# Kernel tuning notes

Measured on AMD Instinct MI355X. Metric: run time of the kernel, lower is better.

## Reference

```python
import jax, jax.numpy as jnp
import numpy as np

B, N, C, H = 8, 1024, 768, 12
HD = C // H
SCALE = HD ** -0.5
LAMBD = 4.0
N_ITERS = 5


def setup_inputs() -> dict:
    key = jax.random.key(0)
    k1, k2, k3, k4, k5 = jax.random.split(key, 5)
    x = jax.random.normal(k1, (B, N, C), dtype=jnp.float32)
    W_qkv = jax.random.normal(k2, (C, 2 * C), dtype=jnp.float32) * (C ** -0.5)
    b_qkv = jax.random.normal(k3, (2 * C,), dtype=jnp.float32) * 0.02
    W_proj = jax.random.normal(k4, (C, C), dtype=jnp.float32) * (C ** -0.5)
    b_proj = jax.random.normal(k5, (C,), dtype=jnp.float32) * 0.02
    return {"x": x, "W_qkv": W_qkv, "b_qkv": b_qkv, "W_proj": W_proj, "b_proj": b_proj}


def _soft_threshold(s, t):
    # (s - t) where s >= t, (s + t) where s <= -t, else 0  (matches the int-mask math)
    return jnp.where(s >= t, s - t, jnp.where(s <= -t, s + t, jnp.zeros_like(s)))


def reference(x, W_qkv, b_qkv, W_proj, b_proj):
    qkv = (x @ W_qkv + b_qkv).reshape(B, N, 2, H, HD)
    qkv = jnp.transpose(qkv, (2, 0, 3, 1, 4))  # [2, B, H, N, HD]
    k, v = qkv[0], qkv[1]

    # mu: [B, H, 1, 1], scalar per (batch, head): N*C/4 / ||k||_1
    mu = (N * C / 4.0) / jnp.sum(jnp.abs(k), axis=(-1, -2), keepdims=True)
    lm = LAMBD * mu

    l = jnp.zeros((B, H, N, HD), dtype=x.dtype)
    y = jnp.zeros((B, H, N, HD), dtype=x.dtype)

    for _ in range(N_ITERS):
        s = _soft_threshold(k - l + y / mu, lm)
        k2 = k - s - y / mu
        attn = jax.nn.softmax(jnp.einsum('bhnd,bhmd->bhnm', k2, k2) * SCALE, axis=-1)
        l = jnp.einsum('bhnm,bhmd->bhnd', attn, v)
        y = y + mu * (k - l - s)

    s = _soft_threshold(k - l + y / mu, lm)
    k2 = k - s - y / mu
    attn = jax.nn.softmax(jnp.einsum('bhnd,bhmd->bhnm', k2, k2) * SCALE, axis=-1)
    out = jnp.einsum('bhnm,bhmd->bhnd', attn, v)  # [B, H, N, HD]

    out = jnp.transpose(out, (0, 2, 1, 3)).reshape(B, N, C)
    out = out @ W_proj + b_proj
    return out, attn
```

## Files before the change

kernel.cpp:

```cpp
#include <hip/hip_runtime.h>

#define B_   8
#define N_   1024
#define C_   768
#define H_   12
#define HD_  64
#define BH_  96
#define SCALE_ 0.125f
#define NIT_ 5

typedef __attribute__((ext_vector_type(8))) short bfrag;
typedef __attribute__((ext_vector_type(4))) float facc;

__device__ __forceinline__ unsigned short bfhi(float x)
{
    return (unsigned short)(__float_as_uint(x) >> 16);
}
__device__ __forceinline__ unsigned short bflo(float x)
{
    const unsigned hu = __float_as_uint(x) & 0xffff0000u;
    return (unsigned short)(__float_as_uint(x - __uint_as_float(hu)) >> 16);
}
__device__ __forceinline__ bfrag pack_hi(float4 a, float4 b)
{
    bfrag r;
    r[0] = (short)bfhi(a.x); r[1] = (short)bfhi(a.y);
    r[2] = (short)bfhi(a.z); r[3] = (short)bfhi(a.w);
    r[4] = (short)bfhi(b.x); r[5] = (short)bfhi(b.y);
    r[6] = (short)bfhi(b.z); r[7] = (short)bfhi(b.w);
    return r;
}
__device__ __forceinline__ bfrag pack_lo(float4 a, float4 b)
{
    bfrag r;
    r[0] = (short)bflo(a.x); r[1] = (short)bflo(a.y);
    r[2] = (short)bflo(a.z); r[3] = (short)bflo(a.w);
    r[4] = (short)bflo(b.x); r[5] = (short)bflo(b.y);
    r[6] = (short)bflo(b.z); r[7] = (short)bflo(b.w);
    return r;
}

__global__ __launch_bounds__(256)
void split_flat(const float* __restrict__ In,
                unsigned short* __restrict__ Oh, unsigned short* __restrict__ Ol)
{
    const size_t i = ((size_t)blockIdx.x * 256 + threadIdx.x) * 8;
    const float4 a = *(const float4*)(In + i);
    const float4 b = *(const float4*)(In + i + 4);
    *(bfrag*)(Oh + i) = pack_hi(a, b);
    *(bfrag*)(Ol + i) = pack_lo(a, b);
}

__global__ __launch_bounds__(256)
void split_wt(const float* __restrict__ W, int ncols,
              unsigned short* __restrict__ Th, unsigned short* __restrict__ Tl)
{
    __shared__ float Ts[64][68];
    const int tid = threadIdx.x;
    const int c0 = blockIdx.x * 64;
    const int k0 = blockIdx.y * 64;

    {
        int e = tid;
#pragma unroll
        for (int t = 0; t < 4; ++t, e += 256) {
            const int r = e >> 4, c4 = (e & 15) << 2;
            *(float4*)&Ts[r][c4] =
                *(const float4*)(W + (size_t)(k0 + r) * ncols + c0 + c4);
        }
    }
    __syncthreads();

#pragma unroll
    for (int t = 0; t < 2; ++t) {
        const int idx = t * 2048 + tid * 8;
        const int cr = idx >> 6, ck = idx & 63;
        bfrag h8, l8;
#pragma unroll
        for (int q = 0; q < 8; ++q) {
            const float v = Ts[ck + q][cr];
            h8[q] = (short)bfhi(v);
            l8[q] = (short)bflo(v);
        }
        const size_t go = (size_t)(c0 + cr) * 768 + k0 + ck;
        *(bfrag*)(Th + go) = h8;
        *(bfrag*)(Tl + go) = l8;
    }
}

__global__ __launch_bounds__(256)
void qkv_mfma(const unsigned short* __restrict__ Xh, const unsigned short* __restrict__ Xl,
              const unsigned short* __restrict__ Wth, const unsigned short* __restrict__ Wtl,
              const float* __restrict__ bias,
              float* __restrict__ Kb, float* __restrict__ Vb)
{
    __shared__ short Ahs[64][72];
    __shared__ short Als[64][72];
    __shared__ short Bhs[64][72];
    __shared__ short Bls[64][72];

    const int tid  = threadIdx.x;
    const int lane = tid & 63;
    const int w    = tid >> 6;
    const int g    = lane >> 4;
    const int r16  = lane & 15;
    const int m0   = blockIdx.y * 64;
    const int c0   = blockIdx.x * 64;

    facc o0 = {0.f, 0.f, 0.f, 0.f};
    facc o1 = {0.f, 0.f, 0.f, 0.f};
    facc o2 = {0.f, 0.f, 0.f, 0.f};
    facc o3 = {0.f, 0.f, 0.f, 0.f};

    const int i0 = tid * 8,        r0 = i0 >> 6, cc0 = i0 & 63;
    const int i1 = 2048 + tid * 8, r1 = i1 >> 6, cc1 = i1 & 63;

    bfrag ta0 = *(const bfrag*)(Xh + (size_t)(m0 + r0) * 768 + cc0);
    bfrag ta1 = *(const bfrag*)(Xh + (size_t)(m0 + r1) * 768 + cc1);
    bfrag tb0 = *(const bfrag*)(Xl + (size_t)(m0 + r0) * 768 + cc0);
    bfrag tb1 = *(const bfrag*)(Xl + (size_t)(m0 + r1) * 768 + cc1);
    bfrag tw0 = *(const bfrag*)(Wth + (size_t)(c0 + r0) * 768 + cc0);
    bfrag tw1 = *(const bfrag*)(Wth + (size_t)(c0 + r1) * 768 + cc1);
    bfrag tz0 = *(const bfrag*)(Wtl + (size_t)(c0 + r0) * 768 + cc0);
    bfrag tz1 = *(const bfrag*)(Wtl + (size_t)(c0 + r1) * 768 + cc1);

    for (int ks = 0; ks < 12; ++ks) {
        __syncthreads();
        *(bfrag*)&Ahs[r0][cc0] = ta0;  *(bfrag*)&Ahs[r1][cc1] = ta1;
        *(bfrag*)&Als[r0][cc0] = tb0;  *(bfrag*)&Als[r1][cc1] = tb1;
        *(bfrag*)&Bhs[r0][cc0] = tw0;  *(bfrag*)&Bhs[r1][cc1] = tw1;
        *(bfrag*)&Bls[r0][cc0] = tz0;  *(bfrag*)&Bls[r1][cc1] = tz1;
        if (ks + 1 < 12) {
            const int kn = (ks + 1) * 64;
            ta0 = *(const bfrag*)(Xh + (size_t)(m0 + r0) * 768 + kn + cc0);
            ta1 = *(const bfrag*)(Xh + (size_t)(m0 + r1) * 768 + kn + cc1);
            tb0 = *(const bfrag*)(Xl + (size_t)(m0 + r0) * 768 + kn + cc0);
            tb1 = *(const bfrag*)(Xl + (size_t)(m0 + r1) * 768 + kn + cc1);
            tw0 = *(const bfrag*)(Wth + (size_t)(c0 + r0) * 768 + kn + cc0);
            tw1 = *(const bfrag*)(Wth + (size_t)(c0 + r1) * 768 + kn + cc1);
            tz0 = *(const bfrag*)(Wtl + (size_t)(c0 + r0) * 768 + kn + cc0);
            tz1 = *(const bfrag*)(Wtl + (size_t)(c0 + r1) * 768 + kn + cc1);
        }
        __syncthreads();

        const bfrag ah0 = *(const bfrag*)&Ahs[16 * w + r16][8 * g];
        const bfrag ah1 = *(const bfrag*)&Ahs[16 * w + r16][32 + 8 * g];
        const bfrag al0 = *(const bfrag*)&Als[16 * w + r16][8 * g];
        const bfrag al1 = *(const bfrag*)&Als[16 * w + r16][32 + 8 * g];
        {
            bfrag b0 = *(const bfrag*)&Bhs[r16][8 * g];
            bfrag b1 = *(const bfrag*)&Bhs[r16][32 + 8 * g];
            bfrag c1 = *(const bfrag*)&Bls[r16][8 * g];
            bfrag c2 = *(const bfrag*)&Bls[r16][32 + 8 * g];
            o0 = __builtin_amdgcn_mfma_f32_16x16x32_bf16(ah0, b0, o0, 0, 0, 0);
            o0 = __builtin_amdgcn_mfma_f32_16x16x32_bf16(al0, b0, o0, 0, 0, 0);
            o0 = __builtin_amdgcn_mfma_f32_16x16x32_bf16(ah0, c1, o0, 0, 0, 0);
            o0 = __builtin_amdgcn_mfma_f32_16x16x32_bf16(ah1, b1, o0, 0, 0, 0);
            o0 = __builtin_amdgcn_mfma_f32_16x16x32_bf16(al1, b1, o0, 0, 0, 0);
            o0 = __builtin_amdgcn_mfma_f32_16x16x32_bf16(ah1, c2, o0, 0, 0, 0);
        }
        {
            bfrag b0 = *(const bfrag*)&Bhs[16 + r16][8 * g];
            bfrag b1 = *(const bfrag*)&Bhs[16 + r16][32 + 8 * g];
            bfrag c1 = *(const bfrag*)&Bls[16 + r16][8 * g];
            bfrag c2 = *(const bfrag*)&Bls[16 + r16][32 + 8 * g];
            o1 = __builtin_amdgcn_mfma_f32_16x16x32_bf16(ah0, b0, o1, 0, 0, 0);
            o1 = __builtin_amdgcn_mfma_f32_16x16x32_bf16(al0, b0, o1, 0, 0, 0);
            o1 = __builtin_amdgcn_mfma_f32_16x16x32_bf16(ah0, c1, o1, 0, 0, 0);
            o1 = __builtin_amdgcn_mfma_f32_16x16x32_bf16(ah1, b1, o1, 0, 0, 0);
            o1 = __builtin_amdgcn_mfma_f32_16x16x32_bf16(al1, b1, o1, 0, 0, 0);
            o1 = __builtin_amdgcn_mfma_f32_16x16x32_bf16(ah1, c2, o1, 0, 0, 0);
        }
        {
            bfrag b0 = *(const bfrag*)&Bhs[32 + r16][8 * g];
            bfrag b1 = *(const bfrag*)&Bhs[32 + r16][32 + 8 * g];
            bfrag c1 = *(const bfrag*)&Bls[32 + r16][8 * g];
            bfrag c2 = *(const bfrag*)&Bls[32 + r16][32 + 8 * g];
            o2 = __builtin_amdgcn_mfma_f32_16x16x32_bf16(ah0, b0, o2, 0, 0, 0);
            o2 = __builtin_amdgcn_mfma_f32_16x16x32_bf16(al0, b0, o2, 0, 0, 0);
            o2 = __builtin_amdgcn_mfma_f32_16x16x32_bf16(ah0, c1, o2, 0, 0, 0);
            o2 = __builtin_amdgcn_mfma_f32_16x16x32_bf16(ah1, b1, o2, 0, 0, 0);
            o2 = __builtin_amdgcn_mfma_f32_16x16x32_bf16(al1, b1, o2, 0, 0, 0);
            o2 = __builtin_amdgcn_mfma_f32_16x16x32_bf16(ah1, c2, o2, 0, 0, 0);
        }
        {
            bfrag b0 = *(const bfrag*)&Bhs[48 + r16][8 * g];
            bfrag b1 = *(const bfrag*)&Bhs[48 + r16][32 + 8 * g];
            bfrag c1 = *(const bfrag*)&Bls[48 + r16][8 * g];
            bfrag c2 = *(const bfrag*)&Bls[48 + r16][32 + 8 * g];
            o3 = __builtin_amdgcn_mfma_f32_16x16x32_bf16(ah0, b0, o3, 0, 0, 0);
            o3 = __builtin_amdgcn_mfma_f32_16x16x32_bf16(al0, b0, o3, 0, 0, 0);
            o3 = __builtin_amdgcn_mfma_f32_16x16x32_bf16(ah0, c1, o3, 0, 0, 0);
            o3 = __builtin_amdgcn_mfma_f32_16x16x32_bf16(ah1, b1, o3, 0, 0, 0);
            o3 = __builtin_amdgcn_mfma_f32_16x16x32_bf16(al1, b1, o3, 0, 0, 0);
            o3 = __builtin_amdgcn_mfma_f32_16x16x32_bf16(ah1, c2, o3, 0, 0, 0);
        }
    }

    const int h = (c0 % C_) >> 6;
    float* tgt = (c0 < C_) ? Kb : Vb;
    const float bb0 = bias[c0 + r16];
    const float bb1 = bias[c0 + 16 + r16];
    const float bb2 = bias[c0 + 32 + r16];
    const float bb3 = bias[c0 + 48 + r16];

    const int mrow = m0 + 16 * w + 4 * g;
    const int bidx = mrow >> 10;
    const int nidx = mrow & 1023;
    float* trow = tgt + ((size_t)(bidx * H_ + h) * N_ + nidx) * HD_ + r16;
    trow[0 * HD_ + 0]  = o0.x + bb0; trow[0 * HD_ + 16] = o1.x + bb1;
    trow[0 * HD_ + 32] = o2.x + bb2; trow[0 * HD_ + 48] = o3.x + bb3;
    trow[1 * HD_ + 0]  = o0.y + bb0; trow[1 * HD_ + 16] = o1.y + bb1;
    trow[1 * HD_ + 32] = o2.y + bb2; trow[1 * HD_ + 48] = o3.y + bb3;
    trow[2 * HD_ + 0]  = o0.z + bb0; trow[2 * HD_ + 16] = o1.z + bb1;
    trow[2 * HD_ + 32] = o2.z + bb2; trow[2 * HD_ + 48] = o3.z + bb3;
    trow[3 * HD_ + 0]  = o0.w + bb0; trow[3 * HD_ + 16] = o1.w + bb1;
    trow[3 * HD_ + 32] = o2.w + bb2; trow[3 * HD_ + 48] = o3.w + bb3;
}

__global__ __launch_bounds__(256)
void proj_mfma(const unsigned short* __restrict__ Lh, const unsigned short* __restrict__ Ll,
               const unsigned short* __restrict__ Wth, const unsigned short* __restrict__ Wtl,
               const float* __restrict__ bias, float* __restrict__ Out)
{
    __shared__ short Ahs[64][72];
    __shared__ short Als[64][72];
    __shared__ short Bhs[64][72];
    __shared__ short Bls[64][72];

    const int tid  = threadIdx.x;
    const int lane = tid & 63;
    const int w    = tid >> 6;
    const int g    = lane >> 4;
    const int r16  = lane & 15;
    const int m0   = blockIdx.y * 64;
    const int c0   = blockIdx.x * 64;

    facc o0 = {0.f, 0.f, 0.f, 0.f};
    facc o1 = {0.f, 0.f, 0.f, 0.f};
    facc o2 = {0.f, 0.f, 0.f, 0.f};
    facc o3 = {0.f, 0.f, 0.f, 0.f};

    const int i0 = tid * 8,        r0 = i0 >> 6, cc0 = i0 & 63;
    const int i1 = 2048 + tid * 8, r1 = i1 >> 6, cc1 = i1 & 63;
    const int t0 = m0 + r0, ab0 = t0 >> 10, an0 = t0 & 1023;
    const int t1 = m0 + r1, ab1 = t1 >> 10, an1 = t1 & 1023;

    bfrag ta0 = *(const bfrag*)(Lh + ((size_t)(ab0 * H_) * N_ + an0) * HD_ + cc0);
    bfrag ta1 = *(const bfrag*)(Lh + ((size_t)(ab1 * H_) * N_ + an1) * HD_ + cc1);
    bfrag tb0 = *(const bfrag*)(Ll + ((size_t)(ab0 * H_) * N_ + an0) * HD_ + cc0);
    bfrag tb1 = *(const bfrag*)(Ll + ((size_t)(ab1 * H_) * N_ + an1) * HD_ + cc1);
    bfrag tw0 = *(const bfrag*)(Wth + (size_t)(c0 + r0) * 768 + cc0);
    bfrag tw1 = *(const bfrag*)(Wth + (size_t)(c0 + r1) * 768 + cc1);
    bfrag tz0 = *(const bfrag*)(Wtl + (size_t)(c0 + r0) * 768 + cc0);
    bfrag tz1 = *(const bfrag*)(Wtl + (size_t)(c0 + r1) * 768 + cc1);

    for (int ks = 0; ks < 12; ++ks) {
        __syncthreads();
        *(bfrag*)&Ahs[r0][cc0] = ta0;  *(bfrag*)&Ahs[r1][cc1] = ta1;
        *(bfrag*)&Als[r0][cc0] = tb0;  *(bfrag*)&Als[r1][cc1] = tb1;
        *(bfrag*)&Bhs[r0][cc0] = tw0;  *(bfrag*)&Bhs[r1][cc1] = tw1;
        *(bfrag*)&Bls[r0][cc0] = tz0;  *(bfrag*)&Bls[r1][cc1] = tz1;
        if (ks + 1 < 12) {
            const int kn = ks + 1;
            const size_t ga0 = ((size_t)(ab0 * H_ + kn) * N_ + an0) * HD_ + cc0;
            const size_t ga1 = ((size_t)(ab1 * H_ + kn) * N_ + an1) * HD_ + cc1;
            ta0 = *(const bfrag*)(Lh + ga0);
            ta1 = *(const bfrag*)(Lh + ga1);
            tb0 = *(const bfrag*)(Ll + ga0);
            tb1 = *(const bfrag*)(Ll + ga1);
            tw0 = *(const bfrag*)(Wth + (size_t)(c0 + r0) * 768 + kn * 64 + cc0);
            tw1 = *(const bfrag*)(Wth + (size_t)(c0 + r1) * 768 + kn * 64 + cc1);
            tz0 = *(const bfrag*)(Wtl + (size_t)(c0 + r0) * 768 + kn * 64 + cc0);
            tz1 = *(const bfrag*)(Wtl + (size_t)(c0 + r1) * 768 + kn * 64 + cc1);
        }
        __syncthreads();

        const bfrag ah0 = *(const bfrag*)&Ahs[16 * w + r16][8 * g];
        const bfrag ah1 = *(const bfrag*)&Ahs[16 * w + r16][32 + 8 * g];
        const bfrag al0 = *(const bfrag*)&Als[16 * w + r16][8 * g];
        const bfrag al1 = *(const bfrag*)&Als[16 * w + r16][32 + 8 * g];
        {
            bfrag b0 = *(const bfrag*)&Bhs[r16][8 * g];
            bfrag b1 = *(const bfrag*)&Bhs[r16][32 + 8 * g];
            bfrag c1 = *(const bfrag*)&Bls[r16][8 * g];
            bfrag c2 = *(const bfrag*)&Bls[r16][32 + 8 * g];
            o0 = __builtin_amdgcn_mfma_f32_16x16x32_bf16(ah0, b0, o0, 0, 0, 0);
            o0 = __builtin_amdgcn_mfma_f32_16x16x32_bf16(al0, b0, o0, 0, 0, 0);
            o0 = __builtin_amdgcn_mfma_f32_16x16x32_bf16(ah0, c1, o0, 0, 0, 0);
            o0 = __builtin_amdgcn_mfma_f32_16x16x32_bf16(ah1, b1, o0, 0, 0, 0);
            o0 = __builtin_amdgcn_mfma_f32_16x16x32_bf16(al1, b1, o0, 0, 0, 0);
            o0 = __builtin_amdgcn_mfma_f32_16x16x32_bf16(ah1, c2, o0, 0, 0, 0);
        }
        {
            bfrag b0 = *(const bfrag*)&Bhs[16 + r16][8 * g];
            bfrag b1 = *(const bfrag*)&Bhs[16 + r16][32 + 8 * g];
            bfrag c1 = *(const bfrag*)&Bls[16 + r16][8 * g];
            bfrag c2 = *(const bfrag*)&Bls[16 + r16][32 + 8 * g];
            o1 = __builtin_amdgcn_mfma_f32_16x16x32_bf16(ah0, b0, o1, 0, 0, 0);
            o1 = __builtin_amdgcn_mfma_f32_16x16x32_bf16(al0, b0, o1, 0, 0, 0);
            o1 = __builtin_amdgcn_mfma_f32_16x16x32_bf16(ah0, c1, o1, 0, 0, 0);
            o1 = __builtin_amdgcn_mfma_f32_16x16x32_bf16(ah1, b1, o1, 0, 0, 0);
            o1 = __builtin_amdgcn_mfma_f32_16x16x32_bf16(al1, b1, o1, 0, 0, 0);
            o1 = __builtin_amdgcn_mfma_f32_16x16x32_bf16(ah1, c2, o1, 0, 0, 0);
        }
        {
            bfrag b0 = *(const bfrag*)&Bhs[32 + r16][8 * g];
            bfrag b1 = *(const bfrag*)&Bhs[32 + r16][32 + 8 * g];
            bfrag c1 = *(const bfrag*)&Bls[32 + r16][8 * g];
            bfrag c2 = *(const bfrag*)&Bls[32 + r16][32 + 8 * g];
            o2 = __builtin_amdgcn_mfma_f32_16x16x32_bf16(ah0, b0, o2, 0, 0, 0);
            o2 = __builtin_amdgcn_mfma_f32_16x16x32_bf16(al0, b0, o2, 0, 0, 0);
            o2 = __builtin_amdgcn_mfma_f32_16x16x32_bf16(ah0, c1, o2, 0, 0, 0);
            o2 = __builtin_amdgcn_mfma_f32_16x16x32_bf16(ah1, b1, o2, 0, 0, 0);
            o2 = __builtin_amdgcn_mfma_f32_16x16x32_bf16(al1, b1, o2, 0, 0, 0);
            o2 = __builtin_amdgcn_mfma_f32_16x16x32_bf16(ah1, c2, o2, 0, 0, 0);
        }
        {
            bfrag b0 = *(const bfrag*)&Bhs[48 + r16][8 * g];
            bfrag b1 = *(const bfrag*)&Bhs[48 + r16][32 + 8 * g];
            bfrag c1 = *(const bfrag*)&Bls[48 + r16][8 * g];
            bfrag c2 = *(const bfrag*)&Bls[48 + r16][32 + 8 * g];
            o3 = __builtin_amdgcn_mfma_f32_16x16x32_bf16(ah0, b0, o3, 0, 0, 0);
            o3 = __builtin_amdgcn_mfma_f32_16x16x32_bf16(al0, b0, o3, 0, 0, 0);
            o3 = __builtin_amdgcn_mfma_f32_16x16x32_bf16(ah0, c1, o3, 0, 0, 0);
            o3 = __builtin_amdgcn_mfma_f32_16x16x32_bf16(ah1, b1, o3, 0, 0, 0);
            o3 = __builtin_amdgcn_mfma_f32_16x16x32_bf16(al1, b1, o3, 0, 0, 0);
            o3 = __builtin_amdgcn_mfma_f32_16x16x32_bf16(ah1, c2, o3, 0, 0, 0);
        }
    }

    const float bb0 = bias[c0 + r16];
    const float bb1 = bias[c0 + 16 + r16];
    const float bb2 = bias[c0 + 32 + r16];
    const float bb3 = bias[c0 + 48 + r16];
    float* orow = Out + (size_t)(m0 + 16 * w + 4 * g) * C_ + c0 + r16;
    orow[0 * C_ + 0]  = o0.x + bb0; orow[0 * C_ + 16] = o1.x + bb1;
    orow[0 * C_ + 32] = o2.x + bb2; orow[0 * C_ + 48] = o3.x + bb3;
    orow[1 * C_ + 0]  = o0.y + bb0; orow[1 * C_ + 16] = o1.y + bb1;
    orow[1 * C_ + 32] = o2.y + bb2; orow[1 * C_ + 48] = o3.y + bb3;
    orow[2 * C_ + 0]  = o0.z + bb0; orow[2 * C_ + 16] = o1.z + bb1;
    orow[2 * C_ + 32] = o2.z + bb2; orow[2 * C_ + 48] = o3.z + bb3;
    orow[3 * C_ + 0]  = o0.w + bb0; orow[3 * C_ + 16] = o1.w + bb1;
    orow[3 * C_ + 32] = o2.w + bb2; orow[3 * C_ + 48] = o3.w + bb3;
}

__global__ __launch_bounds__(256)
void musum(const float* __restrict__ Kb, float* __restrict__ mu)
{
    const int bh = blockIdx.x;
    const int tid = threadIdx.x;
    const float* p = Kb + (size_t)bh * (N_ * HD_);
    float s = 0.0f;
    for (int i = tid; i < N_ * HD_; i += 256) s += fabsf(p[i]);
    for (int off = 32; off; off >>= 1) s += __shfl_down(s, off, 64);
    __shared__ float red[4];
    if ((tid & 63) == 0) red[tid >> 6] = s;
    __syncthreads();
    if (tid == 0)
        mu[bh] = (float)(N_ * C_ / 4.0) / (red[0] + red[1] + red[2] + red[3]);
}

__global__ __launch_bounds__(256)
void ew_fused(const float* __restrict__ Kb, const float* __restrict__ Lb,
              float* __restrict__ Yb, const float* __restrict__ mu,
              float* __restrict__ K2b,
              unsigned short* __restrict__ K2h, unsigned short* __restrict__ K2l,
              int upd)
{
    const int i = blockIdx.x * 256 + threadIdx.x;
    const int bh = i >> 16;
    const float m = mu[bh];
    const float lm = 4.0f * m;
    const float lv = Lb[i];
    float y = Yb[i];
    if (upd) {
        y = 2.0f * y + m * (K2b[i] - lv);
        Yb[i] = y;
    }
    const float yom = y / m;
    const float kv = Kb[i];
    const float t = kv - lv + yom;
    const float s = (t >= lm) ? (t - lm) : ((t <= -lm) ? (t + lm) : 0.0f);
    const float k2 = kv - s - yom;
    K2b[i] = k2;
    K2h[i] = bfhi(k2);
    K2l[i] = bflo(k2);
}

__global__ __launch_bounds__(256)
void vt_split(const float* __restrict__ Vb,
              unsigned short* __restrict__ Vth, unsigned short* __restrict__ Vtl)
{
    __shared__ float Ts[64][68];
    const int tid = threadIdx.x;
    const int bh = blockIdx.y;
    const int n0 = blockIdx.x * 64;
    const float* vb = Vb + ((size_t)bh * N_ + n0) * HD_;

    {
        int e = tid;
#pragma unroll
        for (int t = 0; t < 4; ++t, e += 256) {
            const int r = e >> 4, c4 = (e & 15) << 2;
            *(float4*)&Ts[r][c4] = *(const float4*)(vb + r * HD_ + c4);
        }
    }
    __syncthreads();

#pragma unroll
    for (int t = 0; t < 2; ++t) {
        const int idx = t * 2048 + tid * 8;
        const int d = idx >> 6, c = idx & 63;
        bfrag h8, l8;
#pragma unroll
        for (int q = 0; q < 8; ++q) {
            const float v = Ts[c + q][d];
            h8[q] = (short)bfhi(v);
            l8[q] = (short)bflo(v);
        }
        const size_t go = ((size_t)bh * HD_ + d) * N_ + n0 + c;
        *(bfrag*)(Vth + go) = h8;
        *(bfrag*)(Vtl + go) = l8;
    }
}

__global__ __launch_bounds__(256)
void flash(const unsigned short* __restrict__ K2h, const unsigned short* __restrict__ K2l,
           const unsigned short* __restrict__ Vth, const unsigned short* __restrict__ Vtl,
           float* __restrict__ Lout, float* __restrict__ Mrow, float* __restrict__ Zrow)
{
    __shared__ short Kh[64][72];
    __shared__ short Kl[64][72];
    __shared__ short Vh[64][72];
    __shared__ short Vl[64][72];
    short (&Ph)[64][72] = Kh;
    short (&Pl)[64][72] = Kl;

    const int tid  = threadIdx.x;
    const int lane = tid & 63;
    const int w    = tid >> 6;
    const int g    = lane >> 4;
    const int r16  = lane & 15;
    const int bh   = blockIdx.y;
    const int q0   = blockIdx.x * 64;

    const unsigned short* kh = K2h + (size_t)bh * (N_ * HD_);
    const unsigned short* kl = K2l + (size_t)bh * (N_ * HD_);
    const unsigned short* vh = Vth + (size_t)bh * (N_ * HD_);
    const unsigned short* vl = Vtl + (size_t)bh * (N_ * HD_);

    const size_t qoff = (size_t)(q0 + 16 * w + r16) * HD_ + 8 * g;
    const bfrag qh0 = *(const bfrag*)(kh + qoff);
    const bfrag qh1 = *(const bfrag*)(kh + qoff + 32);
    const bfrag ql0 = *(const bfrag*)(kl + qoff);
    const bfrag ql1 = *(const bfrag*)(kl + qoff + 32);

    const int i0 = tid * 8,        r0 = i0 >> 6, cc0 = i0 & 63;
    const int i1 = 2048 + tid * 8, r1 = i1 >> 6, cc1 = i1 & 63;

    bfrag pk0 = *(const bfrag*)(kh + i0);
    bfrag pk1 = *(const bfrag*)(kh + i1);
    bfrag pm0 = *(const bfrag*)(kl + i0);
    bfrag pm1 = *(const bfrag*)(kl + i1);

    float mr0 = -1e30f, mr1 = -1e30f, mr2 = -1e30f, mr3 = -1e30f;
    float zr0 = 0.0f,  zr1 = 0.0f,  zr2 = 0.0f,  zr3 = 0.0f;
    facc o0 = {0.f, 0.f, 0.f, 0.f};
    facc o1 = {0.f, 0.f, 0.f, 0.f};
    facc o2 = {0.f, 0.f, 0.f, 0.f};
    facc o3 = {0.f, 0.f, 0.f, 0.f};

    for (int kt = 0; kt < 16; ++kt) {
        __syncthreads();
        *(bfrag*)&Kh[r0][cc0] = pk0;  *(bfrag*)&Kh[r1][cc1] = pk1;
        *(bfrag*)&Kl[r0][cc0] = pm0;  *(bfrag*)&Kl[r1][cc1] = pm1;
        const bfrag tv0 = *(const bfrag*)(vh + (size_t)r0 * N_ + kt * 64 + cc0);
        const bfrag tv1 = *(const bfrag*)(vh + (size_t)r1 * N_ + kt * 64 + cc1);
        const bfrag tw0 = *(const bfrag*)(vl + (size_t)r0 * N_ + kt * 64 + cc0);
        const bfrag tw1 = *(const bfrag*)(vl + (size_t)r1 * N_ + kt * 64 + cc1);
        if (kt + 1 < 16) {
            const size_t gn = (size_t)(kt + 1) * 4096;
            pk0 = *(const bfrag*)(kh + gn + i0);
            pk1 = *(const bfrag*)(kh + gn + i1);
            pm0 = *(const bfrag*)(kl + gn + i0);
            pm1 = *(const bfrag*)(kl + gn + i1);
        }
        __syncthreads();

        facc s0 = {0.f, 0.f, 0.f, 0.f};
        facc s1 = {0.f, 0.f, 0.f, 0.f};
        facc s2 = {0.f, 0.f, 0.f, 0.f};
        facc s3 = {0.f, 0.f, 0.f, 0.f};
        {
            bfrag b0 = *(const bfrag*)&Kh[r16][8 * g];
            bfrag b1 = *(const bfrag*)&Kh[r16][32 + 8 * g];
            bfrag c0 = *(const bfrag*)&Kl[r16][8 * g];
            bfrag c1 = *(const bfrag*)&Kl[r16][32 + 8 * g];
            s0 = __builtin_amdgcn_mfma_f32_16x16x32_bf16(qh0, b0, s0, 0, 0, 0);
            s0 = __builtin_amdgcn_mfma_f32_16x16x32_bf16(ql0, b0, s0, 0, 0, 0);
            s0 = __builtin_amdgcn_mfma_f32_16x16x32_bf16(qh0, c0, s0, 0, 0, 0);
            s0 = __builtin_amdgcn_mfma_f32_16x16x32_bf16(qh1, b1, s0, 0, 0, 0);
            s0 = __builtin_amdgcn_mfma_f32_16x16x32_bf16(ql1, b1, s0, 0, 0, 0);
            s0 = __builtin_amdgcn_mfma_f32_16x16x32_bf16(qh1, c1, s0, 0, 0, 0);
        }
        {
            bfrag b0 = *(const bfrag*)&Kh[16 + r16][8 * g];
            bfrag b1 = *(const bfrag*)&Kh[16 + r16][32 + 8 * g];
            bfrag c0 = *(const bfrag*)&Kl[16 + r16][8 * g];
            bfrag c1 = *(const bfrag*)&Kl[16 + r16][32 + 8 * g];
            s1 = __builtin_amdgcn_mfma_f32_16x16x32_bf16(qh0, b0, s1, 0, 0, 0);
            s1 = __builtin_amdgcn_mfma_f32_16x16x32_bf16(ql0, b0, s1, 0, 0, 0);
            s1 = __builtin_amdgcn_mfma_f32_16x16x32_bf16(qh0, c0, s1, 0, 0, 0);
            s1 = __builtin_amdgcn_mfma_f32_16x16x32_bf16(qh1, b1, s1, 0, 0, 0);
            s1 = __builtin_amdgcn_mfma_f32_16x16x32_bf16(ql1, b1, s1, 0, 0, 0);
            s1 = __builtin_amdgcn_mfma_f32_16x16x32_bf16(qh1, c1, s1, 0, 0, 0);
        }
        {
            bfrag b0 = *(const bfrag*)&Kh[32 + r16][8 * g];
            bfrag b1 = *(const bfrag*)&Kh[32 + r16][32 + 8 * g];
            bfrag c0 = *(const bfrag*)&Kl[32 + r16][8 * g];
            bfrag c1 = *(const bfrag*)&Kl[32 + r16][32 + 8 * g];
            s2 = __builtin_amdgcn_mfma_f32_16x16x32_bf16(qh0, b0, s2, 0, 0, 0);
            s2 = __builtin_amdgcn_mfma_f32_16x16x32_bf16(ql0, b0, s2, 0, 0, 0);
            s2 = __builtin_amdgcn_mfma_f32_16x16x32_bf16(qh0, c0, s2, 0, 0, 0);
            s2 = __builtin_amdgcn_mfma_f32_16x16x32_bf16(qh1, b1, s2, 0, 0, 0);
            s2 = __builtin_amdgcn_mfma_f32_16x16x32_bf16(ql1, b1, s2, 0, 0, 0);
            s2 = __builtin_amdgcn_mfma_f32_16x16x32_bf16(qh1, c1, s2, 0, 0, 0);
        }
        {
            bfrag b0 = *(const bfrag*)&Kh[48 + r16][8 * g];
            bfrag b1 = *(const bfrag*)&Kh[48 + r16][32 + 8 * g];
            bfrag c0 = *(const bfrag*)&Kl[48 + r16][8 * g];
            bfrag c1 = *(const bfrag*)&Kl[48 + r16][32 + 8 * g];
            s3 = __builtin_amdgcn_mfma_f32_16x16x32_bf16(qh0, b0, s3, 0, 0, 0);
            s3 = __builtin_amdgcn_mfma_f32_16x16x32_bf16(ql0, b0, s3, 0, 0, 0);
            s3 = __builtin_amdgcn_mfma_f32_16x16x32_bf16(qh0, c0, s3, 0, 0, 0);
            s3 = __builtin_amdgcn_mfma_f32_16x16x32_bf16(qh1, b1, s3, 0, 0, 0);
            s3 = __builtin_amdgcn_mfma_f32_16x16x32_bf16(ql1, b1, s3, 0, 0, 0);
            s3 = __builtin_amdgcn_mfma_f32_16x16x32_bf16(qh1, c1, s3, 0, 0, 0);
        }

        s0 = s0 * SCALE_;  s1 = s1 * SCALE_;  s2 = s2 * SCALE_;  s3 = s3 * SCALE_;

        float mt0 = fmaxf(fmaxf(s0.x, s1.x), fmaxf(s2.x, s3.x));
        float mt1 = fmaxf(fmaxf(s0.y, s1.y), fmaxf(s2.y, s3.y));
        float mt2 = fmaxf(fmaxf(s0.z, s1.z), fmaxf(s2.z, s3.z));
        float mt3 = fmaxf(fmaxf(s0.w, s1.w), fmaxf(s2.w, s3.w));
        for (int off = 8; off; off >>= 1) {
            mt0 = fmaxf(mt0, __shfl_xor(mt0, off, 16));
            mt1 = fmaxf(mt1, __shfl_xor(mt1, off, 16));
            mt2 = fmaxf(mt2, __shfl_xor(mt2, off, 16));
            mt3 = fmaxf(mt3, __shfl_xor(mt3, off, 16));
        }
        const float mn0 = fmaxf(mr0, mt0), mn1 = fmaxf(mr1, mt1);
        const float mn2 = fmaxf(mr2, mt2), mn3 = fmaxf(mr3, mt3);
        const float a0 = __expf(mr0 - mn0), a1 = __expf(mr1 - mn1);
        const float a2 = __expf(mr2 - mn2), a3 = __expf(mr3 - mn3);
        mr0 = mn0; mr1 = mn1; mr2 = mn2; mr3 = mn3;

        const float pa0 = __expf(s0.x - mn0), pa1 = __expf(s0.y - mn1);
        const float pa2 = __expf(s0.z - mn2), pa3 = __expf(s0.w - mn3);
        const float pb0 = __expf(s1.x - mn0), pb1 = __expf(s1.y - mn1);
        const float pb2 = __expf(s1.z - mn2), pb3 = __expf(s1.w - mn3);
        const float pc0 = __expf(s2.x - mn0), pc1 = __expf(s2.y - mn1);
        const float pc2 = __expf(s2.z - mn2), pc3 = __expf(s2.w - mn3);
        const float pd0 = __expf(s3.x - mn0), pd1 = __expf(s3.y - mn1);
        const float pd2 = __expf(s3.z - mn2), pd3 = __expf(s3.w - mn3);

        float zs0 = pa0 + pb0 + pc0 + pd0;
        float zs1 = pa1 + pb1 + pc1 + pd1;
        float zs2 = pa2 + pb2 + pc2 + pd2;
        float zs3 = pa3 + pb3 + pc3 + pd3;
        for (int off = 8; off; off >>= 1) {
            zs0 += __shfl_xor(zs0, off, 16);
            zs1 += __shfl_xor(zs1, off, 16);
            zs2 += __shfl_xor(zs2, off, 16);
            zs3 += __shfl_xor(zs3, off, 16);
        }
        zr0 = zr0 * a0 + zs0;  zr1 = zr1 * a1 + zs1;
        zr2 = zr2 * a2 + zs2;  zr3 = zr3 * a3 + zs3;

        o0.x *= a0; o0.y *= a1; o0.z *= a2; o0.w *= a3;
        o1.x *= a0; o1.y *= a1; o1.z *= a2; o1.w *= a3;
        o2.x *= a0; o2.y *= a1; o2.z *= a2; o2.w *= a3;
        o3.x *= a0; o3.y *= a1; o3.z *= a2; o3.w *= a3;

        *(bfrag*)&Vh[r0][cc0] = tv0;  *(bfrag*)&Vh[r1][cc1] = tv1;
        *(bfrag*)&Vl[r0][cc0] = tw0;  *(bfrag*)&Vl[r1][cc1] = tw1;

        __syncthreads();

        {
            const int pr = 16 * w + 4 * g;
            Ph[pr + 0][r16]      = (short)bfhi(pa0); Pl[pr + 0][r16]      = (short)bflo(pa0);
            Ph[pr + 1][r16]      = (short)bfhi(pa1); Pl[pr + 1][r16]      = (short)bflo(pa1);
            Ph[pr + 2][r16]      = (short)bfhi(pa2); Pl[pr + 2][r16]      = (short)bflo(pa2);
            Ph[pr + 3][r16]      = (short)bfhi(pa3); Pl[pr + 3][r16]      = (short)bflo(pa3);
            Ph[pr + 0][16 + r16] = (short)bfhi(pb0); Pl[pr + 0][16 + r16] = (short)bflo(pb0);
            Ph[pr + 1][16 + r16] = (short)bfhi(pb1); Pl[pr + 1][16 + r16] = (short)bflo(pb1);
            Ph[pr + 2][16 + r16] = (short)bfhi(pb2); Pl[pr + 2][16 + r16] = (short)bflo(pb2);
            Ph[pr + 3][16 + r16] = (short)bfhi(pb3); Pl[pr + 3][16 + r16] = (short)bflo(pb3);
            Ph[pr + 0][32 + r16] = (short)bfhi(pc0); Pl[pr + 0][32 + r16] = (short)bflo(pc0);
            Ph[pr + 1][32 + r16] = (short)bfhi(pc1); Pl[pr + 1][32 + r16] = (short)bflo(pc1);
            Ph[pr + 2][32 + r16] = (short)bfhi(pc2); Pl[pr + 2][32 + r16] = (short)bflo(pc2);
            Ph[pr + 3][32 + r16] = (short)bfhi(pc3); Pl[pr + 3][32 + r16] = (short)bflo(pc3);
            Ph[pr + 0][48 + r16] = (short)bfhi(pd0); Pl[pr + 0][48 + r16] = (short)bflo(pd0);
            Ph[pr + 1][48 + r16] = (short)bfhi(pd1); Pl[pr + 1][48 + r16] = (short)bflo(pd1);
            Ph[pr + 2][48 + r16] = (short)bfhi(pd2); Pl[pr + 2][48 + r16] = (short)bflo(pd2);
            Ph[pr + 3][48 + r16] = (short)bfhi(pd3); Pl[pr + 3][48 + r16] = (short)bflo(pd3);
        }
        __builtin_amdgcn_wave_barrier();

        {
            const bfrag ph0 = *(const bfrag*)&Ph[16 * w + r16][8 * g];
            const bfrag ph1 = *(const bfrag*)&Ph[16 * w + r16][32 + 8 * g];
            const bfrag pl0 = *(const bfrag*)&Pl[16 * w + r16][8 * g];
            const bfrag pl1 = *(const bfrag*)&Pl[16 * w + r16][32 + 8 * g];
            {
                bfrag b0 = *(const bfrag*)&Vh[r16][8 * g];
                bfrag b1 = *(const bfrag*)&Vh[r16][32 + 8 * g];
                bfrag c0 = *(const bfrag*)&Vl[r16][8 * g];
                bfrag c1 = *(const bfrag*)&Vl[r16][32 + 8 * g];
                o0 = __builtin_amdgcn_mfma_f32_16x16x32_bf16(ph0, b0, o0, 0, 0, 0);
                o0 = __builtin_amdgcn_mfma_f32_16x16x32_bf16(pl0, b0, o0, 0, 0, 0);
                o0 = __builtin_amdgcn_mfma_f32_16x16x32_bf16(ph0, c0, o0, 0, 0, 0);
                o0 = __builtin_amdgcn_mfma_f32_16x16x32_bf16(ph1, b1, o0, 0, 0, 0);
                o0 = __builtin_amdgcn_mfma_f32_16x16x32_bf16(pl1, b1, o0, 0, 0, 0);
                o0 = __builtin_amdgcn_mfma_f32_16x16x32_bf16(ph1, c1, o0, 0, 0, 0);
            }
            {
                bfrag b0 = *(const bfrag*)&Vh[16 + r16][8 * g];
                bfrag b1 = *(const bfrag*)&Vh[16 + r16][32 + 8 * g];
                bfrag c0 = *(const bfrag*)&Vl[16 + r16][8 * g];
                bfrag c1 = *(const bfrag*)&Vl[16 + r16][32 + 8 * g];
                o1 = __builtin_amdgcn_mfma_f32_16x16x32_bf16(ph0, b0, o1, 0, 0, 0);
                o1 = __builtin_amdgcn_mfma_f32_16x16x32_bf16(pl0, b0, o1, 0, 0, 0);
                o1 = __builtin_amdgcn_mfma_f32_16x16x32_bf16(ph0, c0, o1, 0, 0, 0);
                o1 = __builtin_amdgcn_mfma_f32_16x16x32_bf16(ph1, b1, o1, 0, 0, 0);
                o1 = __builtin_amdgcn_mfma_f32_16x16x32_bf16(pl1, b1, o1, 0, 0, 0);
                o1 = __builtin_amdgcn_mfma_f32_16x16x32_bf16(ph1, c1, o1, 0, 0, 0);
            }
            {
                bfrag b0 = *(const bfrag*)&Vh[32 + r16][8 * g];
                bfrag b1 = *(const bfrag*)&Vh[32 + r16][32 + 8 * g];
                bfrag c0 = *(const bfrag*)&Vl[32 + r16][8 * g];
                bfrag c1 = *(const bfrag*)&Vl[32 + r16][32 + 8 * g];
                o2 = __builtin_amdgcn_mfma_f32_16x16x32_bf16(ph0, b0, o2, 0, 0, 0);
                o2 = __builtin_amdgcn_mfma_f32_16x16x32_bf16(pl0, b0, o2, 0, 0, 0);
                o2 = __builtin_amdgcn_mfma_f32_16x16x32_bf16(ph0, c0, o2, 0, 0, 0);
                o2 = __builtin_amdgcn_mfma_f32_16x16x32_bf16(ph1, b1, o2, 0, 0, 0);
                o2 = __builtin_amdgcn_mfma_f32_16x16x32_bf16(pl1, b1, o2, 0, 0, 0);
                o2 = __builtin_amdgcn_mfma_f32_16x16x32_bf16(ph1, c1, o2, 0, 0, 0);
            }
            {
                bfrag b0 = *(const bfrag*)&Vh[48 + r16][8 * g];
                bfrag b1 = *(const bfrag*)&Vh[48 + r16][32 + 8 * g];
                bfrag c0 = *(const bfrag*)&Vl[48 + r16][8 * g];
                bfrag c1 = *(const bfrag*)&Vl[48 + r16][32 + 8 * g];
                o3 = __builtin_amdgcn_mfma_f32_16x16x32_bf16(ph0, b0, o3, 0, 0, 0);
                o3 = __builtin_amdgcn_mfma_f32_16x16x32_bf16(pl0, b0, o3, 0, 0, 0);
                o3 = __builtin_amdgcn_mfma_f32_16x16x32_bf16(ph0, c0, o3, 0, 0, 0);
                o3 = __builtin_amdgcn_mfma_f32_16x16x32_bf16(ph1, b1, o3, 0, 0, 0);
                o3 = __builtin_amdgcn_mfma_f32_16x16x32_bf16(pl1, b1, o3, 0, 0, 0);
                o3 = __builtin_amdgcn_mfma_f32_16x16x32_bf16(ph1, c1, o3, 0, 0, 0);
            }
        }
    }

    const float zi0 = 1.0f / zr0, zi1 = 1.0f / zr1;
    const float zi2 = 1.0f / zr2, zi3 = 1.0f / zr3;
    float* lrow = Lout + ((size_t)bh * N_ + q0 + 16 * w + 4 * g) * HD_ + r16;
    lrow[0 * HD_ + 0]  = o0.x * zi0; lrow[0 * HD_ + 16] = o1.x * zi0;
    lrow[0 * HD_ + 32] = o2.x * zi0; lrow[0 * HD_ + 48] = o3.x * zi0;
    lrow[1 * HD_ + 0]  = o0.y * zi1; lrow[1 * HD_ + 16] = o1.y * zi1;
    lrow[1 * HD_ + 32] = o2.y * zi1; lrow[1 * HD_ + 48] = o3.y * zi1;
    lrow[2 * HD_ + 0]  = o0.z * zi2; lrow[2 * HD_ + 16] = o1.z * zi2;
    lrow[2 * HD_ + 32] = o2.z * zi2; lrow[2 * HD_ + 48] = o3.z * zi2;
    lrow[3 * HD_ + 0]  = o0.w * zi3; lrow[3 * HD_ + 16] = o1.w * zi3;
    lrow[3 * HD_ + 32] = o2.w * zi3; lrow[3 * HD_ + 48] = o3.w * zi3;

    if (r16 == 0) {
        const size_t rb = (size_t)bh * N_ + q0 + 16 * w + 4 * g;
        Mrow[rb + 0] = mr0; Mrow[rb + 1] = mr1;
        Mrow[rb + 2] = mr2; Mrow[rb + 3] = mr3;
        Zrow[rb + 0] = zr0; Zrow[rb + 1] = zr1;
        Zrow[rb + 2] = zr2; Zrow[rb + 3] = zr3;
    }
}

__global__ __launch_bounds__(256)
void attn_out_mfma(const float* __restrict__ K2v, const float* __restrict__ Mrow,
                   const float* __restrict__ Zrow, float* __restrict__ A)
{
    __shared__ short Kh[64][72];
    __shared__ short Kl[64][72];

    const int tid  = threadIdx.x;
    const int lane = tid & 63;
    const int w    = tid >> 6;
    const int g    = lane >> 4;
    const int r16  = lane & 15;
    const int bh   = blockIdx.y;
    const int q0   = blockIdx.x * 64;
    const float* k2b = K2v + (size_t)bh * N_ * HD_;

    const int qrow = q0 + 16 * w + r16;
    const float4 f0 = *(const float4*)(k2b + (size_t)qrow * HD_ + 8 * g);
    const float4 f1 = *(const float4*)(k2b + (size_t)qrow * HD_ + 8 * g + 4);
    const float4 f2 = *(const float4*)(k2b + (size_t)qrow * HD_ + 32 + 8 * g);
    const float4 f3 = *(const float4*)(k2b + (size_t)qrow * HD_ + 32 + 8 * g + 4);
    const bfrag qh0 = pack_hi(f0, f1), ql0 = pack_lo(f0, f1);
    const bfrag qh1 = pack_hi(f2, f3), ql1 = pack_lo(f2, f3);

    const size_t mb = (size_t)bh * N_ + q0 + 16 * w + 4 * g;
    const float mi0 = Mrow[mb + 0], mi1 = Mrow[mb + 1];
    const float mi2 = Mrow[mb + 2], mi3 = Mrow[mb + 3];
    const float zi0 = 1.0f / Zrow[mb + 0], zi1 = 1.0f / Zrow[mb + 1];
    const float zi2 = 1.0f / Zrow[mb + 2], zi3 = 1.0f / Zrow[mb + 3];

    const int i0 = tid * 8,        r0 = i0 >> 6, cc0 = i0 & 63;
    const int i1 = 2048 + tid * 8, r1 = i1 >> 6, cc1 = i1 & 63;

    float4 a0 = *(const float4*)(k2b + (size_t)r0 * HD_ + cc0);
    float4 a1 = *(const float4*)(k2b + (size_t)r0 * HD_ + cc0 + 4);
    float4 b0v = *(const float4*)(k2b + (size_t)r1 * HD_ + cc1);
    float4 b1v = *(const float4*)(k2b + (size_t)r1 * HD_ + cc1 + 4);

    for (int kt = 0; kt < 16; ++kt) {
        __syncthreads();
        *(bfrag*)&Kh[r0][cc0] = pack_hi(a0, a1);
        *(bfrag*)&Kl[r0][cc0] = pack_lo(a0, a1);
        *(bfrag*)&Kh[r1][cc1] = pack_hi(b0v, b1v);
        *(bfrag*)&Kl[r1][cc1] = pack_lo(b0v, b1v);
        if (kt + 1 < 16) {
            const size_t gn = (size_t)(kt + 1) * 64;
            a0  = *(const float4*)(k2b + (gn + r0) * HD_ + cc0);
            a1  = *(const float4*)(k2b + (gn + r0) * HD_ + cc0 + 4);
            b0v = *(const float4*)(k2b + (gn + r1) * HD_ + cc1);
            b1v = *(const float4*)(k2b + (gn + r1) * HD_ + cc1 + 4);
        }
        __syncthreads();

        facc s0 = {0.f, 0.f, 0.f, 0.f};
        facc s1 = {0.f, 0.f, 0.f, 0.f};
        facc s2 = {0.f, 0.f, 0.f, 0.f};
        facc s3 = {0.f, 0.f, 0.f, 0.f};
        {
            bfrag b0 = *(const bfrag*)&Kh[r16][8 * g];
            bfrag b1 = *(const bfrag*)&Kh[r16][32 + 8 * g];
            bfrag c0 = *(const bfrag*)&Kl[r16][8 * g];
            bfrag c1 = *(const bfrag*)&Kl[r16][32 + 8 * g];
            s0 = __builtin_amdgcn_mfma_f32_16x16x32_bf16(qh0, b0, s0, 0, 0, 0);
            s0 = __builtin_amdgcn_mfma_f32_16x16x32_bf16(ql0, b0, s0, 0, 0, 0);
            s0 = __builtin_amdgcn_mfma_f32_16x16x32_bf16(qh0, c0, s0, 0, 0, 0);
            s0 = __builtin_amdgcn_mfma_f32_16x16x32_bf16(qh1, b1, s0, 0, 0, 0);
            s0 = __builtin_amdgcn_mfma_f32_16x16x32_bf16(ql1, b1, s0, 0, 0, 0);
            s0 = __builtin_amdgcn_mfma_f32_16x16x32_bf16(qh1, c1, s0, 0, 0, 0);
        }
        {
            bfrag b0 = *(const bfrag*)&Kh[16 + r16][8 * g];
            bfrag b1 = *(const bfrag*)&Kh[16 + r16][32 + 8 * g];
            bfrag c0 = *(const bfrag*)&Kl[16 + r16][8 * g];
            bfrag c1 = *(const bfrag*)&Kl[16 + r16][32 + 8 * g];
            s1 = __builtin_amdgcn_mfma_f32_16x16x32_bf16(qh0, b0, s1, 0, 0, 0);
            s1 = __builtin_amdgcn_mfma_f32_16x16x32_bf16(ql0, b0, s1, 0, 0, 0);
            s1 = __builtin_amdgcn_mfma_f32_16x16x32_bf16(qh0, c0, s1, 0, 0, 0);
            s1 = __builtin_amdgcn_mfma_f32_16x16x32_bf16(qh1, b1, s1, 0, 0, 0);
            s1 = __builtin_amdgcn_mfma_f32_16x16x32_bf16(ql1, b1, s1, 0, 0, 0);
            s1 = __builtin_amdgcn_mfma_f32_16x16x32_bf16(qh1, c1, s1, 0, 0, 0);
        }
        {
            bfrag b0 = *(const bfrag*)&Kh[32 + r16][8 * g];
            bfrag b1 = *(const bfrag*)&Kh[32 + r16][32 + 8 * g];
            bfrag c0 = *(const bfrag*)&Kl[32 + r16][8 * g];
            bfrag c1 = *(const bfrag*)&Kl[32 + r16][32 + 8 * g];
            s2 = __builtin_amdgcn_mfma_f32_16x16x32_bf16(qh0, b0, s2, 0, 0, 0);
            s2 = __builtin_amdgcn_mfma_f32_16x16x32_bf16(ql0, b0, s2, 0, 0, 0);
            s2 = __builtin_amdgcn_mfma_f32_16x16x32_bf16(qh0, c0, s2, 0, 0, 0);
            s2 = __builtin_amdgcn_mfma_f32_16x16x32_bf16(qh1, b1, s2, 0, 0, 0);
            s2 = __builtin_amdgcn_mfma_f32_16x16x32_bf16(ql1, b1, s2, 0, 0, 0);
            s2 = __builtin_amdgcn_mfma_f32_16x16x32_bf16(qh1, c1, s2, 0, 0, 0);
        }
        {
            bfrag b0 = *(const bfrag*)&Kh[48 + r16][8 * g];
            bfrag b1 = *(const bfrag*)&Kh[48 + r16][32 + 8 * g];
            bfrag c0 = *(const bfrag*)&Kl[48 + r16][8 * g];
            bfrag c1 = *(const bfrag*)&Kl[48 + r16][32 + 8 * g];
            s3 = __builtin_amdgcn_mfma_f32_16x16x32_bf16(qh0, b0, s3, 0, 0, 0);
            s3 = __builtin_amdgcn_mfma_f32_16x16x32_bf16(ql0, b0, s3, 0, 0, 0);
            s3 = __builtin_amdgcn_mfma_f32_16x16x32_bf16(qh0, c0, s3, 0, 0, 0);
            s3 = __builtin_amdgcn_mfma_f32_16x16x32_bf16(qh1, b1, s3, 0, 0, 0);
            s3 = __builtin_amdgcn_mfma_f32_16x16x32_bf16(ql1, b1, s3, 0, 0, 0);
            s3 = __builtin_amdgcn_mfma_f32_16x16x32_bf16(qh1, c1, s3, 0, 0, 0);
        }

        s0 = s0 * SCALE_;  s1 = s1 * SCALE_;  s2 = s2 * SCALE_;  s3 = s3 * SCALE_;

        float* ar0 = A + (mb + 0) * N_ + kt * 64;
        float* ar1 = A + (mb + 1) * N_ + kt * 64;
        float* ar2 = A + (mb + 2) * N_ + kt * 64;
        float* ar3 = A + (mb + 3) * N_ + kt * 64;
        ar0[r16]      = __expf(s0.x - mi0) * zi0;
        ar0[16 + r16] = __expf(s1.x - mi0) * zi0;
        ar0[32 + r16] = __expf(s2.x - mi0) * zi0;
        ar0[48 + r16] = __expf(s3.x - mi0) * zi0;
        ar1[r16]      = __expf(s0.y - mi1) * zi1;
        ar1[16 + r16] = __expf(s1.y - mi1) * zi1;
        ar1[32 + r16] = __expf(s2.y - mi1) * zi1;
        ar1[48 + r16] = __expf(s3.y - mi1) * zi1;
        ar2[r16]      = __expf(s0.z - mi2) * zi2;
        ar2[16 + r16] = __expf(s1.z - mi2) * zi2;
        ar2[32 + r16] = __expf(s2.z - mi2) * zi2;
        ar2[48 + r16] = __expf(s3.z - mi2) * zi2;
        ar3[r16]      = __expf(s0.w - mi3) * zi3;
        ar3[16 + r16] = __expf(s1.w - mi3) * zi3;
        ar3[32 + r16] = __expf(s2.w - mi3) * zi3;
        ar3[48 + r16] = __expf(s3.w - mi3) * zi3;
    }
}

extern "C" void kernel_launch(void* const* d_in, const int* in_sizes, int n_in,
                              void* d_out, int out_size, void* d_ws, size_t ws_size,
                              hipStream_t stream)
{
    (void)in_sizes; (void)n_in; (void)out_size; (void)ws_size;

    const float* x  = (const float*)d_in[0];
    const float* Wq = (const float*)d_in[1];
    const float* bq = (const float*)d_in[2];
    const float* Wp = (const float*)d_in[3];
    const float* bp = (const float*)d_in[4];

    float* out_f  = (float*)d_out;
    float* attn_f = out_f + (size_t)B_ * N_ * C_;

    const size_t SZ = (size_t)BH_ * N_ * HD_;
    float* ws   = (float*)d_ws;
    float* kb   = ws;
    float* vb   = ws + SZ;
    float* lb   = ws + 2 * SZ;
    float* yb   = ws + 3 * SZ;
    float* k2b  = ws + 4 * SZ;
    float* mu   = ws + 5 * SZ;
    float* rowm = mu + 128;
    float* rowz = rowm + (size_t)BH_ * N_;

    unsigned short* k2h  = (unsigned short*)attn_f;
    unsigned short* k2l  = k2h + SZ;
    unsigned short* vth  = k2h + 2 * SZ;
    unsigned short* vtl  = k2h + 3 * SZ;
    unsigned short* xh   = k2h + 4 * SZ;
    unsigned short* xl   = k2h + 5 * SZ;
    unsigned short* wqth = k2h + 6 * SZ;
    unsigned short* wqtl = k2h + 7 * SZ;
    unsigned short* wpth = k2h + 8 * SZ;
    unsigned short* wptl = k2h + 9 * SZ;
    unsigned short* lbh  = k2h + 10 * SZ;
    unsigned short* lbl  = k2h + 11 * SZ;

    hipMemsetAsync(lb, 0, SZ * sizeof(float), stream);
    hipMemsetAsync(yb, 0, SZ * sizeof(float), stream);

    split_flat<<<3072, 256, 0, stream>>>(x, xh, xl);
    split_wt<<<dim3(24, 12), 256, 0, stream>>>(Wq, 2 * C_, wqth, wqtl);
    split_wt<<<dim3(12, 12), 256, 0, stream>>>(Wp, C_, wpth, wptl);

    qkv_mfma<<<dim3(24, 128), 256, 0, stream>>>(xh, xl, wqth, wqtl, bq, kb, vb);
    vt_split<<<dim3(16, 96), 256, 0, stream>>>(vb, vth, vtl);
    musum<<<96, 256, 0, stream>>>(kb, mu);

    for (int it = 0; it <= NIT_; ++it) {
        ew_fused<<<24576, 256, 0, stream>>>(kb, lb, yb, mu, k2b, k2h, k2l,
                                            it > 0 ? 1 : 0);
        flash<<<dim3(16, 96), 256, 0, stream>>>(k2h, k2l, vth, vtl, lb, rowm, rowz);
    }

    split_flat<<<3072, 256, 0, stream>>>(lb, lbh, lbl);
    proj_mfma<<<dim3(12, 128), 256, 0, stream>>>(lbh, lbl, wpth, wptl, bp, out_f);
    attn_out_mfma<<<dim3(16, 96), 256, 0, stream>>>(k2b, rowm, rowz, attn_f);
}
```

Before: 1.645 ms.

## Process 128 query rows per flash block and fuse final L split into flash

The flash kernel now computes two 64-row query tiles per workgroup, so each staged K/V tile in shared memory is reused twice and global K/V traffic is halved. The grid shrinks to 8x96 blocks, which raises register pressure and lowers the number of resident blocks. The last iteration writes the bf16 hi/lo split of L directly, removing the separate split_flat launch. The first ew_fused pass zeroes Y and skips reading L and Y, replacing the two memsets.

```diff
diff --git a/kernel.cpp b/kernel.cpp
--- a/kernel.cpp
+++ b/kernel.cpp
@@ -372,17 +372,22 @@
     const int bh = i >> 16;
     const float m = mu[bh];
     const float lm = 4.0f * m;
-    const float lv = Lb[i];
-    float y = Yb[i];
+    const float kv = Kb[i];
+    float k2;
     if (upd) {
-        y = 2.0f * y + m * (K2b[i] - lv);
+        const float lv = Lb[i];
+        const float y = 2.0f * Yb[i] + m * (K2b[i] - lv);
         Yb[i] = y;
-    }
-    const float yom = y / m;
-    const float kv = Kb[i];
-    const float t = kv - lv + yom;
-    const float s = (t >= lm) ? (t - lm) : ((t <= -lm) ? (t + lm) : 0.0f);
-    const float k2 = kv - s - yom;
+        const float yom = y / m;
+        const float t = kv - lv + yom;
+        const float s = (t >= lm) ? (t - lm) : ((t <= -lm) ? (t + lm) : 0.0f);
+        k2 = kv - s - yom;
+    } else {
+        Yb[i] = 0.0f;
+        const float t = kv;
+        const float s = (t >= lm) ? (t - lm) : ((t <= -lm) ? (t + lm) : 0.0f);
+        k2 = kv - s;
+    }
     K2b[i] = k2;
     K2h[i] = bfhi(k2);
     K2l[i] = bflo(k2);
@@ -428,7 +433,8 @@
 __global__ __launch_bounds__(256)
 void flash(const unsigned short* __restrict__ K2h, const unsigned short* __restrict__ K2l,
            const unsigned short* __restrict__ Vth, const unsigned short* __restrict__ Vtl,
-           float* __restrict__ Lout, float* __restrict__ Mrow, float* __restrict__ Zrow)
+           float* __restrict__ Lout, float* __restrict__ Mrow, float* __restrict__ Zrow,
+           unsigned short* __restrict__ Lbh, unsigned short* __restrict__ Lbl, int wsplit)
 {
     __shared__ short Kh[64][72];
     __shared__ short Kl[64][72];
@@ -443,18 +449,23 @@
     const int g    = lane >> 4;
     const int r16  = lane & 15;
     const int bh   = blockIdx.y;
-    const int q0   = blockIdx.x * 64;
+    const int q0   = blockIdx.x * 128;
 
     const unsigned short* kh = K2h + (size_t)bh * (N_ * HD_);
     const unsigned short* kl = K2l + (size_t)bh * (N_ * HD_);
     const unsigned short* vh = Vth + (size_t)bh * (N_ * HD_);
     const unsigned short* vl = Vtl + (size_t)bh * (N_ * HD_);
 
-    const size_t qoff = (size_t)(q0 + 16 * w + r16) * HD_ + 8 * g;
-    const bfrag qh0 = *(const bfrag*)(kh + qoff);
-    const bfrag qh1 = *(const bfrag*)(kh + qoff + 32);
-    const bfrag ql0 = *(const bfrag*)(kl + qoff);
-    const bfrag ql1 = *(const bfrag*)(kl + qoff + 32);
+    const size_t qoffA = (size_t)(q0 + 16 * w + r16) * HD_ + 8 * g;
+    const size_t qoffB = (size_t)(q0 + 64 + 16 * w + r16) * HD_ + 8 * g;
+    const bfrag qhA0 = *(const bfrag*)(kh + qoffA);
+    const bfrag qhA1 = *(const bfrag*)(kh + qoffA + 32);
+    const bfrag qlA0 = *(const bfrag*)(kl + qoffA);
+    const bfrag qlA1 = *(const bfrag*)(kl + qoffA + 32);
+    const bfrag qhB0 = *(const bfrag*)(kh + qoffB);
+    const bfrag qhB1 = *(const bfrag*)(kh + qoffB + 32);
+    const bfrag qlB0 = *(const bfrag*)(kl + qoffB);
+    const bfrag qlB1 = *(const bfrag*)(kl + qoffB + 32);
 
     const int i0 = tid * 8,        r0 = i0 >> 6, cc0 = i0 & 63;
     const int i1 = 2048 + tid * 8, r1 = i1 >> 6, cc1 = i1 & 63;
@@ -464,12 +475,18 @@
     bfrag pm0 = *(const bfrag*)(kl + i0);
     bfrag pm1 = *(const bfrag*)(kl + i1);
 
-    float mr0 = -1e30f, mr1 = -1e30f, mr2 = -1e30f, mr3 = -1e30f;
-    float zr0 = 0.0f,  zr1 = 0.0f,  zr2 = 0.0f,  zr3 = 0.0f;
-    facc o0 = {0.f, 0.f, 0.f, 0.f};
-    facc o1 = {0.f, 0.f, 0.f, 0.f};
-    facc o2 = {0.f, 0.f, 0.f, 0.f};
-    facc o3 = {0.f, 0.f, 0.f, 0.f};
+    float mrA0 = -1e30f, mrA1 = -1e30f, mrA2 = -1e30f, mrA3 = -1e30f;
+    float zrA0 = 0.0f,  zrA1 = 0.0f,  zrA2 = 0.0f,  zrA3 = 0.0f;
+    float mrB0 = -1e30f, mrB1 = -1e30f, mrB2 = -1e30f, mrB3 = -1e30f;
+    float zrB0 = 0.0f,  zrB1 = 0.0f,  zrB2 = 0.0f,  zrB3 = 0.0f;
+    facc oA0 = {0.f, 0.f, 0.f, 0.f};
+    facc oA1 = {0.f, 0.f, 0.f, 0.f};
+    facc oA2 = {0.f, 0.f, 0.f, 0.f};
+    facc oA3 = {0.f, 0.f, 0.f, 0.f};
+    facc oB0 = {0.f, 0.f, 0.f, 0.f};
+    facc oB1 = {0.f, 0.f, 0.f, 0.f};
+    facc oB2 = {0.f, 0.f, 0.f, 0.f};
+    facc oB3 = {0.f, 0.f, 0.f, 0.f};
 
     for (int kt = 0; kt < 16; ++kt) {
         __syncthreads();
@@ -488,130 +505,197 @@
         }
         __syncthreads();
 
-        facc s0 = {0.f, 0.f, 0.f, 0.f};
-        facc s1 = {0.f, 0.f, 0.f, 0.f};
-        facc s2 = {0.f, 0.f, 0.f, 0.f};
-        facc s3 = {0.f, 0.f, 0.f, 0.f};
+        facc sA0 = {0.f, 0.f, 0.f, 0.f};
+        facc sA1 = {0.f, 0.f, 0.f, 0.f};
+        facc sA2 = {0.f, 0.f, 0.f, 0.f};
+        facc sA3 = {0.f, 0.f, 0.f, 0.f};
+        facc sB0 = {0.f, 0.f, 0.f, 0.f};
+        facc sB1 = {0.f, 0.f, 0.f, 0.f};
+        facc sB2 = {0.f, 0.f, 0.f, 0.f};
+        facc sB3 = {0.f, 0.f, 0.f, 0.f};
         {
             bfrag b0 = *(const bfrag*)&Kh[r16][8 * g];
             bfrag b1 = *(const bfrag*)&Kh[r16][32 + 8 * g];
             bfrag c0 = *(const bfrag*)&Kl[r16][8 * g];
             bfrag c1 = *(const bfrag*)&Kl[r16][32 + 8 * g];
-            s0 = __builtin_amdgcn_mfma_f32_16x16x32_bf16(qh0, b0, s0, 0, 0, 0);
-            s0 = __builtin_amdgcn_mfma_f32_16x16x32_bf16(ql0, b0, s0, 0, 0, 0);
-            s0 = __builtin_amdgcn_mfma_f32_16x16x32_bf16(qh0, c0, s0, 0, 0, 0);
-            s0 = __builtin_amdgcn_mfma_f32_16x16x32_bf16(qh1, b1, s0, 0, 0, 0);
-            s0 = __builtin_amdgcn_mfma_f32_16x16x32_bf16(ql1, b1, s0, 0, 0, 0);
-            s0 = __builtin_amdgcn_mfma_f32_16x16x32_bf16(qh1, c1, s0, 0, 0, 0);
+            sA0 = __builtin_amdgcn_mfma_f32_16x16x32_bf16(qhA0, b0, sA0, 0, 0, 0);
+            sA0 = __builtin_amdgcn_mfma_f32_16x16x32_bf16(qlA0, b0, sA0, 0, 0, 0);
+            sA0 = __builtin_amdgcn_mfma_f32_16x16x32_bf16(qhA0, c0, sA0, 0, 0, 0);
+            sA0 = __builtin_amdgcn_mfma_f32_16x16x32_bf16(qhA1, b1, sA0, 0, 0, 0);
+            sA0 = __builtin_amdgcn_mfma_f32_16x16x32_bf16(qlA1, b1, sA0, 0, 0, 0);
+            sA0 = __builtin_amdgcn_mfma_f32_16x16x32_bf16(qhA1, c1, sA0, 0, 0, 0);
+            sB0 = __builtin_amdgcn_mfma_f32_16x16x32_bf16(qhB0, b0, sB0, 0, 0, 0);
+            sB0 = __builtin_amdgcn_mfma_f32_16x16x32_bf16(qlB0, b0, sB0, 0, 0, 0);
+            sB0 = __builtin_amdgcn_mfma_f32_16x16x32_bf16(qhB0, c0, sB0, 0, 0, 0);
+            sB0 = __builtin_amdgcn_mfma_f32_16x16x32_bf16(qhB1, b1, sB0, 0, 0, 0);
+            sB0 = __builtin_amdgcn_mfma_f32_16x16x32_bf16(qlB1, b1, sB0, 0, 0, 0);
+            sB0 = __builtin_amdgcn_mfma_f32_16x16x32_bf16(qhB1, c1, sB0, 0, 0, 0);
         }
         {
             bfrag b0 = *(const bfrag*)&Kh[16 + r16][8 * g];
             bfrag b1 = *(const bfrag*)&Kh[16 + r16][32 + 8 * g];
             bfrag c0 = *(const bfrag*)&Kl[16 + r16][8 * g];
             bfrag c1 = *(const bfrag*)&Kl[16 + r16][32 + 8 * g];
-            s1 = __builtin_amdgcn_mfma_f32_16x16x32_bf16(qh0, b0, s1, 0, 0, 0);
-            s1 = __builtin_amdgcn_mfma_f32_16x16x32_bf16(ql0, b0, s1, 0, 0, 0);
-            s1 = __builtin_amdgcn_mfma_f32_16x16x32_bf16(qh0, c0, s1, 0, 0, 0);
-            s1 = __builtin_amdgcn_mfma_f32_16x16x32_bf16(qh1, b1, s1, 0, 0, 0);
-            s1 = __builtin_amdgcn_mfma_f32_16x16x32_bf16(ql1, b1, s1, 0, 0, 0);
-            s1 = __builtin_amdgcn_mfma_f32_16x16x32_bf16(qh1, c1, s1, 0, 0, 0);
+            sA1 = __builtin_amdgcn_mfma_f32_16x16x32_bf16(qhA0, b0, sA1, 0, 0, 0);
+            sA1 = __builtin_amdgcn_mfma_f32_16x16x32_bf16(qlA0, b0, sA1, 0, 0, 0);
+            sA1 = __builtin_amdgcn_mfma_f32_16x16x32_bf16(qhA0, c0, sA1, 0, 0, 0);
+            sA1 = __builtin_amdgcn_mfma_f32_16x16x32_bf16(qhA1, b1, sA1, 0, 0, 0);
+            sA1 = __builtin_amdgcn_mfma_f32_16x16x32_bf16(qlA1, b1, sA1, 0, 0, 0);
+            sA1 = __builtin_amdgcn_mfma_f32_16x16x32_bf16(qhA1, c1, sA1, 0, 0, 0);
+            sB1 = __builtin_amdgcn_mfma_f32_16x16x32_bf16(qhB0, b0, sB1, 0, 0, 0);
+            sB1 = __builtin_amdgcn_mfma_f32_16x16x32_bf16(qlB0, b0, sB1, 0, 0, 0);
+            sB1 = __builtin_amdgcn_mfma_f32_16x16x32_bf16(qhB0, c0, sB1, 0, 0, 0);
+            sB1 = __builtin_amdgcn_mfma_f32_16x16x32_bf16(qhB1, b1, sB1, 0, 0, 0);
+            sB1 = __builtin_amdgcn_mfma_f32_16x16x32_bf16(qlB1, b1, sB1, 0, 0, 0);
+            sB1 = __builtin_amdgcn_mfma_f32_16x16x32_bf16(qhB1, c1, sB1, 0, 0, 0);
         }
         {
             bfrag b0 = *(const bfrag*)&Kh[32 + r16][8 * g];
             bfrag b1 = *(const bfrag*)&Kh[32 + r16][32 + 8 * g];
             bfrag c0 = *(const bfrag*)&Kl[32 + r16][8 * g];
             bfrag c1 = *(const bfrag*)&Kl[32 + r16][32 + 8 * g];
-            s2 = __builtin_amdgcn_mfma_f32_16x16x32_bf16(qh0, b0, s2, 0, 0, 0);
-            s2 = __builtin_amdgcn_mfma_f32_16x16x32_bf16(ql0, b0, s2, 0, 0, 0);
-            s2 = __builtin_amdgcn_mfma_f32_16x16x32_bf16(qh0, c0, s2, 0, 0, 0);
-            s2 = __builtin_amdgcn_mfma_f32_16x16x32_bf16(qh1, b1, s2, 0, 0, 0);
-            s2 = __builtin_amdgcn_mfma_f32_16x16x32_bf16(ql1, b1, s2, 0, 0, 0);
-            s2 = __builtin_amdgcn_mfma_f32_16x16x32_bf16(qh1, c1, s2, 0, 0, 0);
+            sA2 = __builtin_amdgcn_mfma_f32_16x16x32_bf16(qhA0, b0, sA2, 0, 0, 0);
+            sA2 = __builtin_amdgcn_mfma_f32_16x16x32_bf16(qlA0, b0, sA2, 0, 0, 0);
+            sA2 = __builtin_amdgcn_mfma_f32_16x16x32_bf16(qhA0, c0, sA2, 0, 0, 0);
+            sA2 = __builtin_amdgcn_mfma_f32_16x16x32_bf16(qhA1, b1, sA2, 0, 0, 0);
+            sA2 = __builtin_amdgcn_mfma_f32_16x16x32_bf16(qlA1, b1, sA2, 0, 0, 0);
+            sA2 = __builtin_amdgcn_mfma_f32_16x16x32_bf16(qhA1, c1, sA2, 0, 0, 0);
+            sB2 = __builtin_amdgcn_mfma_f32_16x16x32_bf16(qhB0, b0, sB2, 0, 0, 0);
+            sB2 = __builtin_amdgcn_mfma_f32_16x16x32_bf16(qlB0, b0, sB2, 0, 0, 0);
+            sB2 = __builtin_amdgcn_mfma_f32_16x16x32_bf16(qhB0, c0, sB2, 0, 0, 0);
+            sB2 = __builtin_amdgcn_mfma_f32_16x16x32_bf16(qhB1, b1, sB2, 0, 0, 0);
+            sB2 = __builtin_amdgcn_mfma_f32_16x16x32_bf16(qlB1, b1, sB2, 0, 0, 0);
+            sB2 = __builtin_amdgcn_mfma_f32_16x16x32_bf16(qhB1, c1, sB2, 0, 0, 0);
         }
         {
             bfrag b0 = *(const bfrag*)&Kh[48 + r16][8 * g];
             bfrag b1 = *(const bfrag*)&Kh[48 + r16][32 + 8 * g];
             bfrag c0 = *(const bfrag*)&Kl[48 + r16][8 * g];
             bfrag c1 = *(const bfrag*)&Kl[48 + r16][32 + 8 * g];
-            s3 = __builtin_amdgcn_mfma_f32_16x16x32_bf16(qh0, b0, s3, 0, 0, 0);
-            s3 = __builtin_amdgcn_mfma_f32_16x16x32_bf16(ql0, b0, s3, 0, 0, 0);
-            s3 = __builtin_amdgcn_mfma_f32_16x16x32_bf16(qh0, c0, s3, 0, 0, 0);
-            s3 = __builtin_amdgcn_mfma_f32_16x16x32_bf16(qh1, b1, s3, 0, 0, 0);
-            s3 = __builtin_amdgcn_mfma_f32_16x16x32_bf16(ql1, b1, s3, 0, 0, 0);
-            s3 = __builtin_amdgcn_mfma_f32_16x16x32_bf16(qh1, c1, s3, 0, 0, 0);
-        }
-
-        s0 = s0 * SCALE_;  s1 = s1 * SCALE_;  s2 = s2 * SCALE_;  s3 = s3 * SCALE_;
-
-        float mt0 = fmaxf(fmaxf(s0.x, s1.x), fmaxf(s2.x, s3.x));
-        float mt1 = fmaxf(fmaxf(s0.y, s1.y), fmaxf(s2.y, s3.y));
-        float mt2 = fmaxf(fmaxf(s0.z, s1.z), fmaxf(s2.z, s3.z));
-        float mt3 = fmaxf(fmaxf(s0.w, s1.w), fmaxf(s2.w, s3.w));
+            sA3 = __builtin_amdgcn_mfma_f32_16x16x32_bf16(qhA0, b0, sA3, 0, 0, 0);
+            sA3 = __builtin_amdgcn_mfma_f32_16x16x32_bf16(qlA0, b0, sA3, 0, 0, 0);
+            sA3 = __builtin_amdgcn_mfma_f32_16x16x32_bf16(qhA0, c0, sA3, 0, 0, 0);
+            sA3 = __builtin_amdgcn_mfma_f32_16x16x32_bf16(qhA1, b1, sA3, 0, 0, 0);
+            sA3 = __builtin_amdgcn_mfma_f32_16x16x32_bf16(qlA1, b1, sA3, 0, 0, 0);
+            sA3 = __builtin_amdgcn_mfma_f32_16x16x32_bf16(qhA1, c1, sA3, 0, 0, 0);
+            sB3 = __builtin_amdgcn_mfma_f32_16x16x32_bf16(qhB0, b0, sB3, 0, 0, 0);
+            sB3 = __builtin_amdgcn_mfma_f32_16x16x32_bf16(qlB0, b0, sB3, 0, 0, 0);
+            sB3 = __builtin_amdgcn_mfma_f32_16x16x32_bf16(qhB0, c0, sB3, 0, 0, 0);
+            sB3 = __builtin_amdgcn_mfma_f32_16x16x32_bf16(qhB1, b1, sB3, 0, 0, 0);
+            sB3 = __builtin_amdgcn_mfma_f32_16x16x32_bf16(qlB1, b1, sB3, 0, 0, 0);
+            sB3 = __builtin_amdgcn_mfma_f32_16x16x32_bf16(qhB1, c1, sB3, 0, 0, 0);
+        }
+
+        sA0 = sA0 * SCALE_;  sA1 = sA1 * SCALE_;  sA2 = sA2 * SCALE_;  sA3 = sA3 * SCALE_;
+        sB0 = sB0 * SCALE_;  sB1 = sB1 * SCALE_;  sB2 = sB2 * SCALE_;  sB3 = sB3 * SCALE_;
+
+        float mt0 = fmaxf(fmaxf(sA0.x, sA1.x), fmaxf(sA2.x, sA3.x));
+        float mt1 = fmaxf(fmaxf(sA0.y, sA1.y), fmaxf(sA2.y, sA3.y));
+        float mt2 = fmaxf(fmaxf(sA0.z, sA1.z), fmaxf(sA2.z, sA3.z));
+        float mt3 = fmaxf(fmaxf(sA0.w, sA1.w), fmaxf(sA2.w, sA3.w));
         for (int off = 8; off; off >>= 1) {
             mt0 = fmaxf(mt0, __shfl_xor(mt0, off, 16));
             mt1 = fmaxf(mt1, __shfl_xor(mt1, off, 16));
             mt2 = fmaxf(mt2, __shfl_xor(mt2, off, 16));
             mt3 = fmaxf(mt3, __shfl_xor(mt3, off, 16));
         }
-        const float mn0 = fmaxf(mr0, mt0), mn1 = fmaxf(mr1, mt1);
-        const float mn2 = fmaxf(mr2, mt2), mn3 = fmaxf(mr3, mt3);
-        const float a0 = __expf(mr0 - mn0), a1 = __expf(mr1 - mn1);
-        const float a2 = __expf(mr2 - mn2), a3 = __expf(mr3 - mn3);
-        mr0 = mn0; mr1 = mn1; mr2 = mn2; mr3 = mn3;
-
-        const float pa0 = __expf(s0.x - mn0), pa1 = __expf(s0.y - mn1);
-        const float pa2 = __expf(s0.z - mn2), pa3 = __expf(s0.w - mn3);
-        const float pb0 = __expf(s1.x - mn0), pb1 = __expf(s1.y - mn1);
-        const float pb2 = __expf(s1.z - mn2), pb3 = __expf(s1.w - mn3);
-        const float pc0 = __expf(s2.x - mn0), pc1 = __expf(s2.y - mn1);
-        const float pc2 = __expf(s2.z - mn2), pc3 = __expf(s2.w - mn3);
-        const float pd0 = __expf(s3.x - mn0), pd1 = __expf(s3.y - mn1);
-        const float pd2 = __expf(s3.z - mn2), pd3 = __expf(s3.w - mn3);
-
-        float zs0 = pa0 + pb0 + pc0 + pd0;
-        float zs1 = pa1 + pb1 + pc1 + pd1;
-        float zs2 = pa2 + pb2 + pc2 + pd2;
-        float zs3 = pa3 + pb3 + pc3 + pd3;
+        const float mnA0 = fmaxf(mrA0, mt0), mnA1 = fmaxf(mrA1, mt1);
+        const float mnA2 = fmaxf(mrA2, mt2), mnA3 = fmaxf(mrA3, mt3);
+        const float aA0 = __expf(mrA0 - mnA0), aA1 = __expf(mrA1 - mnA1);
+        const float aA2 = __expf(mrA2 - mnA2), aA3 = __expf(mrA3 - mnA3);
+        mrA0 = mnA0; mrA1 = mnA1; mrA2 = mnA2; mrA3 = mnA3;
+
+        const float paA0 = __expf(sA0.x - mnA0), paA1 = __expf(sA0.y - mnA1);
+        const float paA2 = __expf(sA0.z - mnA2), paA3 = __expf(sA0.w - mnA3);
+        const float pbA0 = __expf(sA1.x - mnA0), pbA1 = __expf(sA1.y - mnA1);
+        const float pbA2 = __expf(sA1.z - mnA2), pbA3 = __expf(sA1.w - mnA3);
+        const float pcA0 = __expf(sA2.x - mnA0), pcA1 = __expf(sA2.y - mnA1);
+        const float pcA2 = __expf(sA2.z - mnA2), pcA3 = __expf(sA2.w - mnA3);
+        const float pdA0 = __expf(sA3.x - mnA0), pdA1 = __expf(sA3.y - mnA1);
+        const float pdA2 = __expf(sA3.z - mnA2), pdA3 = __expf(sA3.w - mnA3);
+
+        float zsA0 = paA0 + pbA0 + pcA0 + pdA0;
+        float zsA1 = paA1 + pbA1 + pcA1 + pdA1;
+        float zsA2 = paA2 + pbA2 + pcA2 + pdA2;
+        float zsA3 = paA3 + pbA3 + pcA3 + pdA3;
         for (int off = 8; off; off >>= 1) {
-            zs0 += __shfl_xor(zs0, off, 16);
-            zs1 += __shfl_xor(zs1, off, 16);
-            zs2 += __shfl_xor(zs2, off, 16);
-            zs3 += __shfl_xor(zs3, off, 16);
-        }
-        zr0 = zr0 * a0 + zs0;  zr1 = zr1 * a1 + zs1;
-        zr2 = zr2 * a2 + zs2;  zr3 = zr3 * a3 + zs3;
-
-        o0.x *= a0; o0.y *= a1; o0.z *= a2; o0.w *= a3;
-        o1.x *= a0; o1.y *= a1; o1.z *= a2; o1.w *= a3;
-        o2.x *= a0; o2.y *= a1; o2.z *= a2; o2.w *= a3;
-        o3.x *= a0; o3.y *= a1; o3.z *= a2; o3.w *= a3;
+            zsA0 += __shfl_xor(zsA0, off, 16);
+            zsA1 += __shfl_xor(zsA1, off, 16);
+            zsA2 += __shfl_xor(zsA2, off, 16);
+            zsA3 += __shfl_xor(zsA3, off, 16);
+        }
+        zrA0 = zrA0 * aA0 + zsA0;  zrA1 = zrA1 * aA1 + zsA1;
+        zrA2 = zrA2 * aA2 + zsA2;  zrA3 = zrA3 * aA3 + zsA3;
+        oA0.x *= aA0; oA0.y *= aA1; oA0.z *= aA2; oA0.w *= aA3;
+        oA1.x *= aA0; oA1.y *= aA1; oA1.z *= aA2; oA1.w *= aA3;
+        oA2.x *= aA0; oA2.y *= aA1; oA2.z *= aA2; oA2.w *= aA3;
+        oA3.x *= aA0; oA3.y *= aA1; oA3.z *= aA2; oA3.w *= aA3;
+
+        mt0 = fmaxf(fmaxf(sB0.x, sB1.x), fmaxf(sB2.x, sB3.x));
+        mt1 = fmaxf(fmaxf(sB0.y, sB1.y), fmaxf(sB2.y, sB3.y));
+        mt2 = fmaxf(fmaxf(sB0.z, sB1.z), fmaxf(sB2.z, sB3.z));
+        mt3 = fmaxf(fmaxf(sB0.w, sB1.w), fmaxf(sB2.w, sB3.w));
+        for (int off = 8; off; off >>= 1) {
+            mt0 = fmaxf(mt0, __shfl_xor(mt0, off, 16));
+            mt1 = fmaxf(mt1, __shfl_xor(mt1, off, 16));
+            mt2 = fmaxf(mt2, __shfl_xor(mt2, off, 16));
+            mt3 = fmaxf(mt3, __shfl_xor(mt3, off, 16));
+        }
+        const float mnB0 = fmaxf(mrB0, mt0), mnB1 = fmaxf(mrB1, mt1);
+        const float mnB2 = fmaxf(mrB2, mt2), mnB3 = fmaxf(mrB3, mt3);
+        const float aB0 = __expf(mrB0 - mnB0), aB1 = __expf(mrB1 - mnB1);
+        const float aB2 = __expf(mrB2 - mnB2), aB3 = __expf(mrB3 - mnB3);
+        mrB0 = mnB0; mrB1 = mnB1; mrB2 = mnB2; mrB3 = mnB3;
+
+        const float paB0 = __expf(sB0.x - mnB0), paB1 = __expf(sB0.y - mnB1);
+        const float paB2 = __expf(sB0.z - mnB2), paB3 = __expf(sB0.w - mnB3);
+        const float pbB0 = __expf(sB1.x - mnB0), pbB1 = __expf(sB1.y - mnB1);
+        const float pbB2 = __expf(sB1.z - mnB2), pbB3 = __expf(sB1.w - mnB3);
+        const float pcB0 = __expf(sB2.x - mnB0), pcB1 = __expf(sB2.y - mnB1);
+        const float pcB2 = __expf(sB2.z - mnB2), pcB3 = __expf(sB2.w - mnB3);
+        const float pdB0 = __expf(sB3.x - mnB0), pdB1 = __expf(sB3.y - mnB1);
+        const float pdB2 = __expf(sB3.z - mnB2), pdB3 = __expf(sB3.w - mnB3);
+
+        float zsB0 = paB0 + pbB0 + pcB0 + pdB0;
+        float zsB1 = paB1 + pbB1 + pcB1 + pdB1;
+        float zsB2 = paB2 + pbB2 + pcB2 + pdB2;
+        float zsB3 = paB3 + pbB3 + pcB3 + pdB3;
+        for (int off = 8; off; off >>= 1) {
+            zsB0 += __shfl_xor(zsB0, off, 16);
+            zsB1 += __shfl_xor(zsB1, off, 16);
+            zsB2 += __shfl_xor(zsB2, off, 16);
+            zsB3 += __shfl_xor(zsB3, off, 16);
+        }
+        zrB0 = zrB0 * aB0 + zsB0;  zrB1 = zrB1 * aB1 + zsB1;
+        zrB2 = zrB2 * aB2 + zsB2;  zrB3 = zrB3 * aB3 + zsB3;
+        oB0.x *= aB0; oB0.y *= aB1; oB0.z *= aB2; oB0.w *= aB3;
+        oB1.x *= aB0; oB1.y *= aB1; oB1.z *= aB2; oB1.w *= aB3;
+        oB2.x *= aB0; oB2.y *= aB1; oB2.z *= aB2; oB2.w *= aB3;
+        oB3.x *= aB0; oB3.y *= aB1; oB3.z *= aB2; oB3.w *= aB3;
 
         *(bfrag*)&Vh[r0][cc0] = tv0;  *(bfrag*)&Vh[r1][cc1] = tv1;
         *(bfrag*)&Vl[r0][cc0] = tw0;  *(bfrag*)&Vl[r1][cc1] = tw1;
 
         __syncthreads();
 
-        {
-            const int pr = 16 * w + 4 * g;
-            Ph[pr + 0][r16]      = (short)bfhi(pa0); Pl[pr + 0][r16]      = (short)bflo(pa0);
-            Ph[pr + 1][r16]      = (short)bfhi(pa1); Pl[pr + 1][r16]      = (short)bflo(pa1);
-            Ph[pr + 2][r16]      = (short)bfhi(pa2); Pl[pr + 2][r16]      = (short)bflo(pa2);
-            Ph[pr + 3][r16]      = (short)bfhi(pa3); Pl[pr + 3][r16]      = (short)bflo(pa3);
-            Ph[pr + 0][16 + r16] = (short)bfhi(pb0); Pl[pr + 0][16 + r16] = (short)bflo(pb0);
-            Ph[pr + 1][16 + r16] = (short)bfhi(pb1); Pl[pr + 1][16 + r16] = (short)bflo(pb1);
-            Ph[pr + 2][16 + r16] = (short)bfhi(pb2); Pl[pr + 2][16 + r16] = (short)bflo(pb2);
-            Ph[pr + 3][16 + r16] = (short)bfhi(pb3); Pl[pr + 3][16 + r16] = (short)bflo(pb3);
-            Ph[pr + 0][32 + r16] = (short)bfhi(pc0); Pl[pr + 0][32 + r16] = (short)bflo(pc0);
-            Ph[pr + 1][32 + r16] = (short)bfhi(pc1); Pl[pr + 1][32 + r16] = (short)bflo(pc1);
-            Ph[pr + 2][32 + r16] = (short)bfhi(pc2); Pl[pr + 2][32 + r16] = (short)bflo(pc2);
-            Ph[pr + 3][32 + r16] = (short)bfhi(pc3); Pl[pr + 3][32 + r16] = (short)bflo(pc3);
-            Ph[pr + 0][48 + r16] = (short)bfhi(pd0); Pl[pr + 0][48 + r16] = (short)bflo(pd0);
-            Ph[pr + 1][48 + r16] = (short)bfhi(pd1); Pl[pr + 1][48 + r16] = (short)bflo(pd1);
-            Ph[pr + 2][48 + r16] = (short)bfhi(pd2); Pl[pr + 2][48 + r16] = (short)bflo(pd2);
-            Ph[pr + 3][48 + r16] = (short)bfhi(pd3); Pl[pr + 3][48 + r16] = (short)bflo(pd3);
-        }
+        const int pr = 16 * w + 4 * g;
+        Ph[pr + 0][r16]      = (short)bfhi(paA0); Pl[pr + 0][r16]      = (short)bflo(paA0);
+        Ph[pr + 1][r16]      = (short)bfhi(paA1); Pl[pr + 1][r16]      = (short)bflo(paA1);
+        Ph[pr + 2][r16]      = (short)bfhi(paA2); Pl[pr + 2][r16]      = (short)bflo(paA2);
+        Ph[pr + 3][r16]      = (short)bfhi(paA3); Pl[pr + 3][r16]      = (short)bflo(paA3);
+        Ph[pr + 0][16 + r16] = (short)bfhi(pbA0); Pl[pr + 0][16 + r16] = (short)bflo(pbA0);
+        Ph[pr + 1][16 + r16] = (short)bfhi(pbA1); Pl[pr + 1][16 + r16] = (short)bflo(pbA1);
+        Ph[pr + 2][16 + r16] = (short)bfhi(pbA2); Pl[pr + 2][16 + r16] = (short)bflo(pbA2);
+        Ph[pr + 3][16 + r16] = (short)bfhi(pbA3); Pl[pr + 3][16 + r16] = (short)bflo(pbA3);
+        Ph[pr + 0][32 + r16] = (short)bfhi(pcA0); Pl[pr + 0][32 + r16] = (short)bflo(pcA0);
+        Ph[pr + 1][32 + r16] = (short)bfhi(pcA1); Pl[pr + 1][32 + r16] = (short)bflo(pcA1);
+        Ph[pr + 2][32 + r16] = (short)bfhi(pcA2); Pl[pr + 2][32 + r16] = (short)bflo(pcA2);
+        Ph[pr + 3][32 + r16] = (short)bfhi(pcA3); Pl[pr + 3][32 + r16] = (short)bflo(pcA3);
+        Ph[pr + 0][48 + r16] = (short)bfhi(pdA0); Pl[pr + 0][48 + r16] = (short)bflo(pdA0);
+        Ph[pr + 1][48 + r16] = (short)bfhi(pdA1); Pl[pr + 1][48 + r16] = (short)bflo(pdA1);
+        Ph[pr + 2][48 + r16] = (short)bfhi(pdA2); Pl[pr + 2][48 + r16] = (short)bflo(pdA2);
+        Ph[pr + 3][48 + r16] = (short)bfhi(pdA3); Pl[pr + 3][48 + r16] = (short)bflo(pdA3);
         __builtin_amdgcn_wave_barrier();
-
         {
             const bfrag ph0 = *(const bfrag*)&Ph[16 * w + r16][8 * g];
             const bfrag ph1 = *(const bfrag*)&Ph[16 * w + r16][32 + 8 * g];
@@ -622,70 +706,202 @@
                 bfrag b1 = *(const bfrag*)&Vh[r16][32 + 8 * g];
                 bfrag c0 = *(const bfrag*)&Vl[r16][8 * g];
                 bfrag c1 = *(const bfrag*)&Vl[r16][32 + 8 * g];
-                o0 = __builtin_amdgcn_mfma_f32_16x16x32_bf16(ph0, b0, o0, 0, 0, 0);
-                o0 = __builtin_amdgcn_mfma_f32_16x16x32_bf16(pl0, b0, o0, 0, 0, 0);
-                o0 = __builtin_amdgcn_mfma_f32_16x16x32_bf16(ph0, c0, o0, 0, 0, 0);
-                o0 = __builtin_amdgcn_mfma_f32_16x16x32_bf16(ph1, b1, o0, 0, 0, 0);
-                o0 = __builtin_amdgcn_mfma_f32_16x16x32_bf16(pl1, b1, o0, 0, 0, 0);
-                o0 = __builtin_amdgcn_mfma_f32_16x16x32_bf16(ph1, c1, o0, 0, 0, 0);
+                oA0 = __builtin_amdgcn_mfma_f32_16x16x32_bf16(ph0, b0, oA0, 0, 0, 0);
+                oA0 = __builtin_amdgcn_mfma_f32_16x16x32_bf16(pl0, b0, oA0, 0, 0, 0);
+                oA0 = __builtin_amdgcn_mfma_f32_16x16x32_bf16(ph0, c0, oA0, 0, 0, 0);
+                oA0 = __builtin_amdgcn_mfma_f32_16x16x32_bf16(ph1, b1, oA0, 0, 0, 0);
+                oA0 = __builtin_amdgcn_mfma_f32_16x16x32_bf16(pl1, b1, oA0, 0, 0, 0);
+                oA0 = __builtin_amdgcn_mfma_f32_16x16x32_bf16(ph1, c1, oA0, 0, 0, 0);
             }
             {
                 bfrag b0 = *(const bfrag*)&Vh[16 + r16][8 * g];
                 bfrag b1 = *(const bfrag*)&Vh[16 + r16][32 + 8 * g];
                 bfrag c0 = *(const bfrag*)&Vl[16 + r16][8 * g];
                 bfrag c1 = *(const bfrag*)&Vl[16 + r16][32 + 8 * g];
-                o1 = __builtin_amdgcn_mfma_f32_16x16x32_bf16(ph0, b0, o1, 0, 0, 0);
-                o1 = __builtin_amdgcn_mfma_f32_16x16x32_bf16(pl0, b0, o1, 0, 0, 0);
-                o1 = __builtin_amdgcn_mfma_f32_16x16x32_bf16(ph0, c0, o1, 0, 0, 0);
-                o1 = __builtin_amdgcn_mfma_f32_16x16x32_bf16(ph1, b1, o1, 0, 0, 0);
-                o1 = __builtin_amdgcn_mfma_f32_16x16x32_bf16(pl1, b1, o1, 0, 0, 0);
-                o1 = __builtin_amdgcn_mfma_f32_16x16x32_bf16(ph1, c1, o1, 0, 0, 0);
+                oA1 = __builtin_amdgcn_mfma_f32_16x16x32_bf16(ph0, b0, oA1, 0, 0, 0);
+                oA1 = __builtin_amdgcn_mfma_f32_16x16x32_bf16(pl0, b0, oA1, 0, 0, 0);
+                oA1 = __builtin_amdgcn_mfma_f32_16x16x32_bf16(ph0, c0, oA1, 0, 0, 0);
+                oA1 = __builtin_amdgcn_mfma_f32_16x16x32_bf16(ph1, b1, oA1, 0, 0, 0);
+                oA1 = __builtin_amdgcn_mfma_f32_16x16x32_bf16(pl1, b1, oA1, 0, 0, 0);
+                oA1 = __builtin_amdgcn_mfma_f32_16x16x32_bf16(ph1, c1, oA1, 0, 0, 0);
             }
             {
                 bfrag b0 = *(const bfrag*)&Vh[32 + r16][8 * g];
                 bfrag b1 = *(const bfrag*)&Vh[32 + r16][32 + 8 * g];
                 bfrag c0 = *(const bfrag*)&Vl[32 + r16][8 * g];
                 bfrag c1 = *(const bfrag*)&Vl[32 + r16][32 + 8 * g];
-                o2 = __builtin_amdgcn_mfma_f32_16x16x32_bf16(ph0, b0, o2, 0, 0, 0);
-                o2 = __builtin_amdgcn_mfma_f32_16x16x32_bf16(pl0, b0, o2, 0, 0, 0);
-                o2 = __builtin_amdgcn_mfma_f32_16x16x32_bf16(ph0, c0, o2, 0, 0, 0);
-                o2 = __builtin_amdgcn_mfma_f32_16x16x32_bf16(ph1, b1, o2, 0, 0, 0);
-                o2 = __builtin_amdgcn_mfma_f32_16x16x32_bf16(pl1, b1, o2, 0, 0, 0);
-                o2 = __builtin_amdgcn_mfma_f32_16x16x32_bf16(ph1, c1, o2, 0, 0, 0);
+                oA2 = __builtin_amdgcn_mfma_f32_16x16x32_bf16(ph0, b0, oA2, 0, 0, 0);
+                oA2 = __builtin_amdgcn_mfma_f32_16x16x32_bf16(pl0, b0, oA2, 0, 0, 0);
+                oA2 = __builtin_amdgcn_mfma_f32_16x16x32_bf16(ph0, c0, oA2, 0, 0, 0);
+                oA2 = __builtin_amdgcn_mfma_f32_16x16x32_bf16(ph1, b1, oA2, 0, 0, 0);
+                oA2 = __builtin_amdgcn_mfma_f32_16x16x32_bf16(pl1, b1, oA2, 0, 0, 0);
+                oA2 = __builtin_amdgcn_mfma_f32_16x16x32_bf16(ph1, c1, oA2, 0, 0, 0);
             }
             {
                 bfrag b0 = *(const bfrag*)&Vh[48 + r16][8 * g];
                 bfrag b1 = *(const bfrag*)&Vh[48 + r16][32 + 8 * g];
                 bfrag c0 = *(const bfrag*)&Vl[48 + r16][8 * g];
                 bfrag c1 = *(const bfrag*)&Vl[48 + r16][32 + 8 * g];
-                o3 = __builtin_amdgcn_mfma_f32_16x16x32_bf16(ph0, b0, o3, 0, 0, 0);
-                o3 = __builtin_amdgcn_mfma_f32_16x16x32_bf16(pl0, b0, o3, 0, 0, 0);
-                o3 = __builtin_amdgcn_mfma_f32_16x16x32_bf16(ph0, c0, o3, 0, 0, 0);
-                o3 = __builtin_amdgcn_mfma_f32_16x16x32_bf16(ph1, b1, o3, 0, 0, 0);
-                o3 = __builtin_amdgcn_mfma_f32_16x16x32_bf16(pl1, b1, o3, 0, 0, 0);
-                o3 = __builtin_amdgcn_mfma_f32_16x16x32_bf16(ph1, c1, o3, 0, 0, 0);
+                oA3 = __builtin_amdgcn_mfma_f32_16x16x32_bf16(ph0, b0, oA3, 0, 0, 0);
+                oA3 = __builtin_amdgcn_mfma_f32_16x16x32_bf16(pl0, b0, oA3, 0, 0, 0);
+                oA3 = __builtin_amdgcn_mfma_f32_16x16x32_bf16(ph0, c0, oA3, 0, 0, 0);
+                oA3 = __builtin_amdgcn_mfma_f32_16x16x32_bf16(ph1, b1, oA3, 0, 0, 0);
+                oA3 = __builtin_amdgcn_mfma_f32_16x16x32_bf16(pl1, b1, oA3, 0, 0, 0);
+                oA3 = __builtin_amdgcn_mfma_f32_16x16x32_bf16(ph1, c1, oA3, 0, 0, 0);
             }
         }
-    }
-
-    const float zi0 = 1.0f / zr0, zi1 = 1.0f / zr1;
-    const float zi2 = 1.0f / zr2, zi3 = 1.0f / zr3;
-    float* lrow = Lout + ((size_t)bh * N_ + q0 + 16 * w + 4 * g) * HD_ + r16;
-    lrow[0 * HD_ + 0]  = o0.x * zi0; lrow[0 * HD_ + 16] = o1.x * zi0;
-    lrow[0 * HD_ + 32] = o2.x * zi0; lrow[0 * HD_ + 48] = o3.x * zi0;
-    lrow[1 * HD_ + 0]  = o0.y * zi1; lrow[1 * HD_ + 16] = o1.y * zi1;
-    lrow[1 * HD_ + 32] = o2.y * zi1; lrow[1 * HD_ + 48] = o3.y * zi1;
-    lrow[2 * HD_ + 0]  = o0.z * zi2; lrow[2 * HD_ + 16] = o1.z * zi2;
-    lrow[2 * HD_ + 32] = o2.z * zi2; lrow[2 * HD_ + 48] = o3.z * zi2;
-    lrow[3 * HD_ + 0]  = o0.w * zi3; lrow[3 * HD_ + 16] = o1.w * zi3;
-    lrow[3 * HD_ + 32] = o2.w * zi3; lrow[3 * HD_ + 48] = o3.w * zi3;
-
-    if (r16 == 0) {
-        const size_t rb = (size_t)bh * N_ + q0 + 16 * w + 4 * g;
-        Mrow[rb + 0] = mr0; Mrow[rb + 1] = mr1;
-        Mrow[rb + 2] = mr2; Mrow[rb + 3] = mr3;
-        Zrow[rb + 0] = zr0; Zrow[rb + 1] = zr1;
-        Zrow[rb + 2] = zr2; Zrow[rb + 3] = zr3;
+        __builtin_amdgcn_wave_barrier();
+
+        Ph[pr + 0][r16]      = (short)bfhi(paB0); Pl[pr + 0][r16]      = (short)bflo(paB0);
+        Ph[pr + 1][r16]      = (short)bfhi(paB1); Pl[pr + 1][r16]      = (short)bflo(paB1);
+        Ph[pr + 2][r16]      = (short)bfhi(paB2); Pl[pr + 2][r16]      = (short)bflo(paB2);
+        Ph[pr + 3][r16]      = (short)bfhi(paB3); Pl[pr + 3][r16]      = (short)bflo(paB3);
+        Ph[pr + 0][16 + r16] = (short)bfhi(pbB0); Pl[pr + 0][16 + r16] = (short)bflo(pbB0);
+        Ph[pr + 1][16 + r16] = (short)bfhi(pbB1); Pl[pr + 1][16 + r16] = (short)bflo(pbB1);
+        Ph[pr + 2][16 + r16] = (short)bfhi(pbB2); Pl[pr + 2][16 + r16] = (short)bflo(pbB2);
+        Ph[pr + 3][16 + r16] = (short)bfhi(pbB3); Pl[pr + 3][16 + r16] = (short)bflo(pbB3);
+        Ph[pr + 0][32 + r16] = (short)bfhi(pcB0); Pl[pr + 0][32 + r16] = (short)bflo(pcB0);
+        Ph[pr + 1][32 + r16] = (short)bfhi(pcB1); Pl[pr + 1][32 + r16] = (short)bflo(pcB1);
+        Ph[pr + 2][32 + r16] = (short)bfhi(pcB2); Pl[pr + 2][32 + r16] = (short)bflo(pcB2);
+        Ph[pr + 3][32 + r16] = (short)bfhi(pcB3); Pl[pr + 3][32 + r16] = (short)bflo(pcB3);
+        Ph[pr + 0][48 + r16] = (short)bfhi(pdB0); Pl[pr + 0][48 + r16] = (short)bflo(pdB0);
+        Ph[pr + 1][48 + r16] = (short)bfhi(pdB1); Pl[pr + 1][48 + r16] = (short)bflo(pdB1);
+        Ph[pr + 2][48 + r16] = (short)bfhi(pdB2); Pl[pr + 2][48 + r16] = (short)bflo(pdB2);
+        Ph[pr + 3][48 + r16] = (short)bfhi(pdB3); Pl[pr + 3][48 + r16] = (short)bflo(pdB3);
+        __builtin_amdgcn_wave_barrier();
+        {
+            const bfrag ph0 = *(const bfrag*)&Ph[16 * w + r16][8 * g];
+            const bfrag ph1 = *(const bfrag*)&Ph[16 * w + r16][32 + 8 * g];
+            const bfrag pl0 = *(const bfrag*)&Pl[16 * w + r16][8 * g];
+            const bfrag pl1 = *(const bfrag*)&Pl[16 * w + r16][32 + 8 * g];
+            {
+                bfrag b0 = *(const bfrag*)&Vh[r16][8 * g];
+                bfrag b1 = *(const bfrag*)&Vh[r16][32 + 8 * g];
+                bfrag c0 = *(const bfrag*)&Vl[r16][8 * g];
+                bfrag c1 = *(const bfrag*)&Vl[r16][32 + 8 * g];
+                oB0 = __builtin_amdgcn_mfma_f32_16x16x32_bf16(ph0, b0, oB0, 0, 0, 0);
+                oB0 = __builtin_amdgcn_mfma_f32_16x16x32_bf16(pl0, b0, oB0, 0, 0, 0);
+                oB0 = __builtin_amdgcn_mfma_f32_16x16x32_bf16(ph0, c0, oB0, 0, 0, 0);
+                oB0 = __builtin_amdgcn_mfma_f32_16x16x32_bf16(ph1, b1, oB0, 0, 0, 0);
+                oB0 = __builtin_amdgcn_mfma_f32_16x16x32_bf16(pl1, b1, oB0, 0, 0, 0);
+                oB0 = __builtin_amdgcn_mfma_f32_16x16x32_bf16(ph1, c1, oB0, 0, 0, 0);
+            }
+            {
+                bfrag b0 = *(const bfrag*)&Vh[16 + r16][8 * g];
+                bfrag b1 = *(const bfrag*)&Vh[16 + r16][32 + 8 * g];
+                bfrag c0 = *(const bfrag*)&Vl[16 + r16][8 * g];
+                bfrag c1 = *(const bfrag*)&Vl[16 + r16][32 + 8 * g];
+                oB1 = __builtin_amdgcn_mfma_f32_16x16x32_bf16(ph0, b0, oB1, 0, 0, 0);
+                oB1 = __builtin_amdgcn_mfma_f32_16x16x32_bf16(pl0, b0, oB1, 0, 0, 0);
+                oB1 = __builtin_amdgcn_mfma_f32_16x16x32_bf16(ph0, c0, oB1, 0, 0, 0);
+                oB1 = __builtin_amdgcn_mfma_f32_16x16x32_bf16(ph1, b1, oB1, 0, 0, 0);
+                oB1 = __builtin_amdgcn_mfma_f32_16x16x32_bf16(pl1, b1, oB1, 0, 0, 0);
+                oB1 = __builtin_amdgcn_mfma_f32_16x16x32_bf16(ph1, c1, oB1, 0, 0, 0);
+            }
+            {
+                bfrag b0 = *(const bfrag*)&Vh[32 + r16][8 * g];
+                bfrag b1 = *(const bfrag*)&Vh[32 + r16][32 + 8 * g];
+                bfrag c0 = *(const bfrag*)&Vl[32 + r16][8 * g];
+                bfrag c1 = *(const bfrag*)&Vl[32 + r16][32 + 8 * g];
+                oB2 = __builtin_amdgcn_mfma_f32_16x16x32_bf16(ph0, b0, oB2, 0, 0, 0);
+                oB2 = __builtin_amdgcn_mfma_f32_16x16x32_bf16(pl0, b0, oB2, 0, 0, 0);
+                oB2 = __builtin_amdgcn_mfma_f32_16x16x32_bf16(ph0, c0, oB2, 0, 0, 0);
+                oB2 = __builtin_amdgcn_mfma_f32_16x16x32_bf16(ph1, b1, oB2, 0, 0, 0);
+                oB2 = __builtin_amdgcn_mfma_f32_16x16x32_bf16(pl1, b1, oB2, 0, 0, 0);
+                oB2 = __builtin_amdgcn_mfma_f32_16x16x32_bf16(ph1, c1, oB2, 0, 0, 0);
+            }
+            {
+                bfrag b0 = *(const bfrag*)&Vh[48 + r16][8 * g];
+                bfrag b1 = *(const bfrag*)&Vh[48 + r16][32 + 8 * g];
+                bfrag c0 = *(const bfrag*)&Vl[48 + r16][8 * g];
+                bfrag c1 = *(const bfrag*)&Vl[48 + r16][32 + 8 * g];
+                oB3 = __builtin_amdgcn_mfma_f32_16x16x32_bf16(ph0, b0, oB3, 0, 0, 0);
+                oB3 = __builtin_amdgcn_mfma_f32_16x16x32_bf16(pl0, b0, oB3, 0, 0, 0);
+                oB3 = __builtin_amdgcn_mfma_f32_16x16x32_bf16(ph0, c0, oB3, 0, 0, 0);
+                oB3 = __builtin_amdgcn_mfma_f32_16x16x32_bf16(ph1, b1, oB3, 0, 0, 0);
+                oB3 = __builtin_amdgcn_mfma_f32_16x16x32_bf16(pl1, b1, oB3, 0, 0, 0);
+                oB3 = __builtin_amdgcn_mfma_f32_16x16x32_bf16(ph1, c1, oB3, 0, 0, 0);
+            }
+        }
+    }
+
+    {
+        const float zi0 = 1.0f / zrA0, zi1 = 1.0f / zrA1;
+        const float zi2 = 1.0f / zrA2, zi3 = 1.0f / zrA3;
+        const size_t base = ((size_t)bh * N_ + q0 + 16 * w + 4 * g) * HD_ + r16;
+        float* lrow = Lout + base;
+        const float v00 = oA0.x * zi0, v01 = oA1.x * zi0, v02 = oA2.x * zi0, v03 = oA3.x * zi0;
+        const float v10 = oA0.y * zi1, v11 = oA1.y * zi1, v12 = oA2.y * zi1, v13 = oA3.y * zi1;
+        const float v20 = oA0.z * zi2, v21 = oA1.z * zi2, v22 = oA2.z * zi2, v23 = oA3.z * zi2;
+        const float v30 = oA0.w * zi3, v31 = oA1.w * zi3, v32 = oA2.w * zi3, v33 = oA3.w * zi3;
+        lrow[0 * HD_ + 0] = v00; lrow[0 * HD_ + 16] = v01; lrow[0 * HD_ + 32] = v02; lrow[0 * HD_ + 48] = v03;
+        lrow[1 * HD_ + 0] = v10; lrow[1 * HD_ + 16] = v11; lrow[1 * HD_ + 32] = v12; lrow[1 * HD_ + 48] = v13;
+        lrow[2 * HD_ + 0] = v20; lrow[2 * HD_ + 16] = v21; lrow[2 * HD_ + 32] = v22; lrow[2 * HD_ + 48] = v23;
+        lrow[3 * HD_ + 0] = v30; lrow[3 * HD_ + 16] = v31; lrow[3 * HD_ + 32] = v32; lrow[3 * HD_ + 48] = v33;
+        if (wsplit) {
+            Lbh[base + 0 * HD_ + 0] = bfhi(v00); Lbl[base + 0 * HD_ + 0] = bflo(v00);
+            Lbh[base + 0 * HD_ + 16] = bfhi(v01); Lbl[base + 0 * HD_ + 16] = bflo(v01);
+            Lbh[base + 0 * HD_ + 32] = bfhi(v02); Lbl[base + 0 * HD_ + 32] = bflo(v02);
+            Lbh[base + 0 * HD_ + 48] = bfhi(v03); Lbl[base + 0 * HD_ + 48] = bflo(v03);
+            Lbh[base + 1 * HD_ + 0] = bfhi(v10); Lbl[base + 1 * HD_ + 0] = bflo(v10);
+            Lbh[base + 1 * HD_ + 16] = bfhi(v11); Lbl[base + 1 * HD_ + 16] = bflo(v11);
+            Lbh[base + 1 * HD_ + 32] = bfhi(v12); Lbl[base + 1 * HD_ + 32] = bflo(v12);
+            Lbh[base + 1 * HD_ + 48] = bfhi(v13); Lbl[base + 1 * HD_ + 48] = bflo(v13);
+            Lbh[base + 2 * HD_ + 0] = bfhi(v20); Lbl[base + 2 * HD_ + 0] = bflo(v20);
+            Lbh[base + 2 * HD_ + 16] = bfhi(v21); Lbl[base + 2 * HD_ + 16] = bflo(v21);
+            Lbh[base + 2 * HD_ + 32] = bfhi(v22); Lbl[base + 2 * HD_ + 32] = bflo(v22);
+            Lbh[base + 2 * HD_ + 48] = bfhi(v23); Lbl[base + 2 * HD_ + 48] = bflo(v23);
+            Lbh[base + 3 * HD_ + 0] = bfhi(v30); Lbl[base + 3 * HD_ + 0] = bflo(v30);
+            Lbh[base + 3 * HD_ + 16] = bfhi(v31); Lbl[base + 3 * HD_ + 16] = bflo(v31);
+            Lbh[base + 3 * HD_ + 32] = bfhi(v32); Lbl[base + 3 * HD_ + 32] = bflo(v32);
+            Lbh[base + 3 * HD_ + 48] = bfhi(v33); Lbl[base + 3 * HD_ + 48] = bflo(v33);
+        }
+        if (r16 == 0) {
+            const size_t rb = (size_t)bh * N_ + q0 + 16 * w + 4 * g;
+            Mrow[rb + 0] = mrA0; Mrow[rb + 1] = mrA1;
+            Mrow[rb + 2] = mrA2; Mrow[rb + 3] = mrA3;
+            Zrow[rb + 0] = zrA0; Zrow[rb + 1] = zrA1;
+            Zrow[rb + 2] = zrA2; Zrow[rb + 3] = zrA3;
+        }
+    }
+    {
+        const float zi0 = 1.0f / zrB0, zi1 = 1.0f / zrB1;
+        const float zi2 = 1.0f / zrB2, zi3 = 1.0f / zrB3;
+        const size_t base = ((size_t)bh * N_ + q0 + 64 + 16 * w + 4 * g) * HD_ + r16;
+        float* lrow = Lout + base;
+        const float v00 = oB0.x * zi0, v01 = oB1.x * zi0, v02 = oB2.x * zi0, v03 = oB3.x * zi0;
+        const float v10 = oB0.y * zi1, v11 = oB1.y * zi1, v12 = oB2.y * zi1, v13 = oB3.y * zi1;
+        const float v20 = oB0.z * zi2, v21 = oB1.z * zi2, v22 = oB2.z * zi2, v23 = oB3.z * zi2;
+        const float v30 = oB0.w * zi3, v31 = oB1.w * zi3, v32 = oB2.w * zi3, v33 = oB3.w * zi3;
+        lrow[0 * HD_ + 0] = v00; lrow[0 * HD_ + 16] = v01; lrow[0 * HD_ + 32] = v02; lrow[0 * HD_ + 48] = v03;
+        lrow[1 * HD_ + 0] = v10; lrow[1 * HD_ + 16] = v11; lrow[1 * HD_ + 32] = v12; lrow[1 * HD_ + 48] = v13;
+        lrow[2 * HD_ + 0] = v20; lrow[2 * HD_ + 16] = v21; lrow[2 * HD_ + 32] = v22; lrow[2 * HD_ + 48] = v23;
+        lrow[3 * HD_ + 0] = v30; lrow[3 * HD_ + 16] = v31; lrow[3 * HD_ + 32] = v32; lrow[3 * HD_ + 48] = v33;
+        if (wsplit) {
+            Lbh[base + 0 * HD_ + 0] = bfhi(v00); Lbl[base + 0 * HD_ + 0] = bflo(v00);
+            Lbh[base + 0 * HD_ + 16] = bfhi(v01); Lbl[base + 0 * HD_ + 16] = bflo(v01);
+            Lbh[base + 0 * HD_ + 32] = bfhi(v02); Lbl[base + 0 * HD_ + 32] = bflo(v02);
+            Lbh[base + 0 * HD_ + 48] = bfhi(v03); Lbl[base + 0 * HD_ + 48] = bflo(v03);
+            Lbh[base + 1 * HD_ + 0] = bfhi(v10); Lbl[base + 1 * HD_ + 0] = bflo(v10);
+            Lbh[base + 1 * HD_ + 16] = bfhi(v11); Lbl[base + 1 * HD_ + 16] = bflo(v11);
+            Lbh[base + 1 * HD_ + 32] = bfhi(v12); Lbl[base + 1 * HD_ + 32] = bflo(v12);
+            Lbh[base + 1 * HD_ + 48] = bfhi(v13); Lbl[base + 1 * HD_ + 48] = bflo(v13);
+            Lbh[base + 2 * HD_ + 0] = bfhi(v20); Lbl[base + 2 * HD_ + 0] = bflo(v20);
+            Lbh[base + 2 * HD_ + 16] = bfhi(v21); Lbl[base + 2 * HD_ + 16] = bflo(v21);
+            Lbh[base + 2 * HD_ + 32] = bfhi(v22); Lbl[base + 2 * HD_ + 32] = bflo(v22);
+            Lbh[base + 2 * HD_ + 48] = bfhi(v23); Lbl[base + 2 * HD_ + 48] = bflo(v23);
+            Lbh[base + 3 * HD_ + 0] = bfhi(v30); Lbl[base + 3 * HD_ + 0] = bflo(v30);
+            Lbh[base + 3 * HD_ + 16] = bfhi(v31); Lbl[base + 3 * HD_ + 16] = bflo(v31);
+            Lbh[base + 3 * HD_ + 32] = bfhi(v32); Lbl[base + 3 * HD_ + 32] = bflo(v32);
+            Lbh[base + 3 * HD_ + 48] = bfhi(v33); Lbl[base + 3 * HD_ + 48] = bflo(v33);
+        }
+        if (r16 == 0) {
+            const size_t rb = (size_t)bh * N_ + q0 + 64 + 16 * w + 4 * g;
+            Mrow[rb + 0] = mrB0; Mrow[rb + 1] = mrB1;
+            Mrow[rb + 2] = mrB2; Mrow[rb + 3] = mrB3;
+            Zrow[rb + 0] = zrB0; Zrow[rb + 1] = zrB1;
+            Zrow[rb + 2] = zrB2; Zrow[rb + 3] = zrB3;
+        }
     }
 }
 
@@ -859,9 +1075,6 @@
     unsigned short* lbh  = k2h + 10 * SZ;
     unsigned short* lbl  = k2h + 11 * SZ;
 
-    hipMemsetAsync(lb, 0, SZ * sizeof(float), stream);
-    hipMemsetAsync(yb, 0, SZ * sizeof(float), stream);
-
     split_flat<<<3072, 256, 0, stream>>>(x, xh, xl);
     split_wt<<<dim3(24, 12), 256, 0, stream>>>(Wq, 2 * C_, wqth, wqtl);
     split_wt<<<dim3(12, 12), 256, 0, stream>>>(Wp, C_, wpth, wptl);
@@ -873,10 +1086,10 @@
     for (int it = 0; it <= NIT_; ++it) {
         ew_fused<<<24576, 256, 0, stream>>>(kb, lb, yb, mu, k2b, k2h, k2l,
                                             it > 0 ? 1 : 0);
-        flash<<<dim3(16, 96), 256, 0, stream>>>(k2h, k2l, vth, vtl, lb, rowm, rowz);
-    }
-
-    split_flat<<<3072, 256, 0, stream>>>(lb, lbh, lbl);
+        flash<<<dim3(8, 96), 256, 0, stream>>>(k2h, k2l, vth, vtl, lb, rowm, rowz,
+                                               lbh, lbl, it == NIT_ ? 1 : 0);
+    }
+
     proj_mfma<<<dim3(12, 128), 256, 0, stream>>>(lbh, lbl, wpth, wptl, bp, out_f);
     attn_out_mfma<<<dim3(16, 96), 256, 0, stream>>>(k2b, rowm, rowz, attn_f);
 }
```

Result: no change. 1.629 ms (-1.0%).
